# Kernel optimization log

Hardware: AMD Instinct MI355X
Metric: run time of the kernel (lower is better)

Reference implementation:

```python
import jax, jax.numpy as jnp
import numpy as np

B, C, S, H, W = 1, 256, 64, 32, 128
BLOCKS, HEADS, DH = 2, 8, 32
SCALE = DH ** (-0.5)


def layer_norm(x, w, b, eps=1e-5):
    mu = jnp.mean(x, axis=-1, keepdims=True)
    var = jnp.var(x, axis=-1, keepdims=True)
    return (x - mu) * jax.lax.rsqrt(var + eps) * w + b


def generate_y_for_attn(y, u):
    # y: (B,C,H,W), u: (B,S,S) float -> (B, S^2, 2H, C)
    Bv, Cv, Hv, Wv = y.shape
    Sv = u.shape[1]
    uf = jnp.floor(u).reshape(Bv, Sv * Sv)
    u_left = jnp.clip(uf, 0, Wv - 1).astype(jnp.int32)
    u_right = jnp.clip(uf + 1, 0, Wv - 1).astype(jnp.int32)
    yf = y.reshape(Bv, Cv * Hv, Wv)

    def gather_w(idx):
        idxb = jnp.broadcast_to(idx[:, None, :], (Bv, Cv * Hv, Sv * Sv))
        return jnp.take_along_axis(yf, idxb, axis=2).reshape(Bv, Cv, Hv, Sv * Sv)

    ys = jnp.concatenate([gather_w(u_left), gather_w(u_right)], axis=2)  # (B,C,2H,S2)
    return ys.transpose(0, 3, 2, 1)  # (B, S2, 2H, C)


def cross_attention(x, y, p, i):
    # x: (B,M,C), y: (B,M,N,C)
    q = layer_norm(x, p['ln_q_w'][i], p['ln_q_b'][i]) @ p['Wq'][i]        # (B,M,HD)
    k = layer_norm(y, p['ln_k_w'][i], p['ln_k_b'][i]) @ p['Wk'][i]        # (B,M,N,HD)
    v = layer_norm(y, p['ln_v_w'][i], p['ln_v_b'][i]) @ p['Wv'][i]        # (B,M,N,HD)
    Bv, M, _ = q.shape
    N = k.shape[2]
    q = q.reshape(Bv, M, HEADS, DH)
    k = k.reshape(Bv, M, N, HEADS, DH)
    v = v.reshape(Bv, M, N, HEADS, DH)
    dot = SCALE * jnp.einsum('bmhd,bmnhd->bhmn', q, k)                    # (B,H,M,N)
    attn = jax.nn.softmax(dot, axis=-1)
    a = jnp.einsum('bhmn,bmnhd->bmhd', attn, v).reshape(Bv, M, HEADS * DH)
    z = a @ p['Wproj'][i] + p['bproj'][i]
    z = layer_norm(z, p['ln_pre_w'][i], p['ln_pre_b'][i])
    h = jax.nn.gelu(z @ p['Wm1'][i] + p['bm1'][i], approximate=False)
    z = z + (h @ p['Wm2'][i] + p['bm2'][i])
    return layer_norm(z, p['ln_post_w'][i], p['ln_post_b'][i])


def setup_inputs() -> dict:
    key = jax.random.key(0)
    ks = jax.random.split(key, 16)
    std = 0.02
    inp = {
        'grd2sat': jax.random.normal(ks[0], (B, C, S, S), jnp.float32),
        'grd_x': jax.random.normal(ks[1], (B, C, H, W), jnp.float32),
        'u': jax.random.uniform(ks[2], (B, S, S), jnp.float32) * (W - 1),
        'ln_q_w': jnp.ones((BLOCKS, C)), 'ln_q_b': jnp.zeros((BLOCKS, C)),
        'ln_k_w': jnp.ones((BLOCKS, C)), 'ln_k_b': jnp.zeros((BLOCKS, C)),
        'ln_v_w': jnp.ones((BLOCKS, C)), 'ln_v_b': jnp.zeros((BLOCKS, C)),
        'Wq': std * jax.random.normal(ks[3], (BLOCKS, C, HEADS * DH)),
        'Wk': std * jax.random.normal(ks[4], (BLOCKS, C, HEADS * DH)),
        'Wv': std * jax.random.normal(ks[5], (BLOCKS, C, HEADS * DH)),
        'Wproj': std * jax.random.normal(ks[6], (BLOCKS, HEADS * DH, C)),
        'bproj': jnp.zeros((BLOCKS, C)),
        'ln_pre_w': jnp.ones((BLOCKS, C)), 'ln_pre_b': jnp.zeros((BLOCKS, C)),
        'Wm1': std * jax.random.normal(ks[7], (BLOCKS, C, 2 * C)),
        'bm1': jnp.zeros((BLOCKS, 2 * C)),
        'Wm2': std * jax.random.normal(ks[8], (BLOCKS, 2 * C, C)),
        'bm2': jnp.zeros((BLOCKS, C)),
        'ln_post_w': jnp.ones((BLOCKS, C)), 'ln_post_b': jnp.zeros((BLOCKS, C)),
    }
    return inp


def reference(grd2sat, grd_x, u, ln_q_w, ln_q_b, ln_k_w, ln_k_b, ln_v_w, ln_v_b,
              Wq, Wk, Wv, Wproj, bproj, ln_pre_w, ln_pre_b, Wm1, bm1, Wm2, bm2,
              ln_post_w, ln_post_b):
    p = dict(ln_q_w=ln_q_w, ln_q_b=ln_q_b, ln_k_w=ln_k_w, ln_k_b=ln_k_b,
             ln_v_w=ln_v_w, ln_v_b=ln_v_b, Wq=Wq, Wk=Wk, Wv=Wv, Wproj=Wproj,
             bproj=bproj, ln_pre_w=ln_pre_w, ln_pre_b=ln_pre_b, Wm1=Wm1, bm1=bm1,
             Wm2=Wm2, bm2=bm2, ln_post_w=ln_post_w, ln_post_b=ln_post_b)
    y_attn = generate_y_for_attn(grd_x, u)               # (B, S^2, 2H, C)
    x = grd2sat.reshape(B, C, S * S).transpose(0, 2, 1)  # (B, M, C)
    for i in range(BLOCKS):
        # (Swin self-attention layer omitted; cross-attention stack only.)
        x = cross_attention(x, y_attn, p, i)
    out = x.transpose(0, 2, 1).reshape(B, C, S, S)
    # L2 normalize over channel dim
    norm = jnp.sqrt(jnp.sum(out * out, axis=1, keepdims=True))
    return out / jnp.maximum(norm, 1e-12)
```

## Files before the change

### kernel.cpp

```cpp
#include <hip/hip_runtime.h>
#include <math.h>


#define C_DIM 256
#define M_DIM 4096
#define W_DIM 128
#define H_DIM 32
#define ATT_SCALE 0.17677669529663687f

typedef __attribute__((ext_vector_type(8))) short short8;
typedef __attribute__((ext_vector_type(4))) short short4v;
typedef __attribute__((ext_vector_type(4))) float floatx4;

__device__ __forceinline__ unsigned short f2bf(float f) {
    unsigned u = __float_as_uint(f);
    unsigned r = (u + 0x7fffu + ((u >> 16) & 1u)) >> 16;
    return (unsigned short)r;
}
__device__ __forceinline__ float gelu_exact(float x) {
    return 0.5f * x * (1.0f + erff(x * 0.70710678118654752f));
}

struct PrepArgs {
    const float* grd2sat; float* xcur;
    const float* grd_x;   float* yhat;
    const float* u; int* perm; int4* chunks; int* nchunks;
    const float* win[12]; unsigned short* wout[12]; const float* wlnw[12];
    int wR[12], wC[12], wbase[13];
    const float* fW[10]; const float* flnb[10]; const float* fbase[10];
    float* fout[10];
    int fN[10], fwcol[10], focol[10];
};

__global__ __launch_bounds__(256) void prep_kernel(PrepArgs a) {
    __shared__ float smemf[9024];
    int b = blockIdx.x, t = threadIdx.x;
    if (b < 256) {
        float (*tile)[65] = (float(*)[65])smemf;
        int m0 = (b & 63) << 6, c0 = (b >> 6) << 6;
        for (int it = 0; it < 16; ++it) {
            int idx = it * 256 + t;
            int co = idx >> 6, mo = idx & 63;
            tile[co][mo] = a.grd2sat[(size_t)(c0 + co) * M_DIM + m0 + mo];
        }
        __syncthreads();
        for (int it = 0; it < 16; ++it) {
            int idx = it * 256 + t;
            int mo = idx >> 6, co = idx & 63;
            a.xcur[(size_t)(m0 + mo) * C_DIM + c0 + co] = tile[co][mo];
        }
    } else if (b < 384) {
        int idx = b - 256;
        int h = idx & 31, w0 = (idx >> 5) << 5;
        float (*tile)[33] = (float(*)[33])smemf;
        float (*ps)[32] = (float(*)[32])(smemf + 8448);
        float (*pss)[32] = (float(*)[32])(smemf + 8704);
        float* mu_s = smemf + 8960;
        float* rs_s = smemf + 8992;
        int wo = t & 31, cb = t >> 5;
        for (int it = 0; it < 32; ++it) {
            int c = it * 8 + cb;
            tile[c][wo] = a.grd_x[(size_t)c * (H_DIM * W_DIM) + h * W_DIM + w0 + wo];
        }
        __syncthreads();
        {
            int w = t & 31, part = t >> 5;
            float s = 0.f, ss = 0.f;
            for (int c = part * 32; c < part * 32 + 32; ++c) {
                float x = tile[c][w];
                s += x; ss += x * x;
            }
            ps[part][w] = s; pss[part][w] = ss;
        }
        __syncthreads();
        if (t < 32) {
            float s = 0.f, ss = 0.f;
            for (int p = 0; p < 8; ++p) { s += ps[p][t]; ss += pss[p][t]; }
            float mu = s * (1.f / 256.f);
            float var = ss * (1.f / 256.f) - mu * mu;
            mu_s[t] = mu;
            rs_s[t] = rsqrtf(var + 1e-5f);
        }
        __syncthreads();
        for (int jj = 0; jj < 32; ++jj) {
            float mu = mu_s[jj], rs = rs_s[jj];
            a.yhat[((size_t)(w0 + jj) * H_DIM + h) * C_DIM + t] =
                (tile[t][jj] - mu) * rs;
        }
    } else if (b < 1408) {
        int wI = b - 384;
        int e = 0;
        while (wI >= a.wbase[e + 1]) ++e;
        int tl = wI - a.wbase[e];
        int tilesC = a.wC[e] >> 5;
        int tr = tl / tilesC, tc = tl - tr * tilesC;
        int r0 = tr << 5, c0 = tc << 5;
        const float* in = a.win[e];
        unsigned short* out = a.wout[e];
        const float* lnw = a.wlnw[e];
        int R = a.wR[e], Cc = a.wC[e];
        float (*tile)[33] = (float(*)[33])smemf;
        int rl = t >> 3, cq = (t & 7) << 2;
        float4 v = *(const float4*)&in[(size_t)(r0 + rl) * Cc + c0 + cq];
        if (lnw) {
            float s = lnw[r0 + rl];
            v.x *= s; v.y *= s; v.z *= s; v.w *= s;
        }
        tile[rl][cq + 0] = v.x;
        tile[rl][cq + 1] = v.y;
        tile[rl][cq + 2] = v.z;
        tile[rl][cq + 3] = v.w;
        __syncthreads();
        int cl = t >> 3, rq = (t & 7) << 2;
        ushort4 o;
        o.x = f2bf(tile[rq + 0][cl]);
        o.y = f2bf(tile[rq + 1][cl]);
        o.z = f2bf(tile[rq + 2][cl]);
        o.w = f2bf(tile[rq + 3][cl]);
        *(ushort4*)&out[(size_t)(c0 + cl) * R + r0 + rq] = o;
    } else if (b < 1448) {
        int idx = b - 1408;
        int jj = idx >> 2, part = idx & 3;
        int N = a.fN[jj];
        int c = t & 63, kp = t >> 6;
        int wcol = a.fwcol[jj] + (part << 6) + c;
        const float* W = a.fW[jj];
        const float* lb = a.flnb[jj];
        float s = 0.f;
        for (int k = kp * 64; k < kp * 64 + 64; ++k)
            s += lb[k] * W[(size_t)k * N + wcol];
        smemf[(kp << 6) + c] = s;
        __syncthreads();
        if (t < 64) {
            float tot = smemf[t] + smemf[64 + t] + smemf[128 + t] + smemf[192 + t];
            int ocol = a.focol[jj] + (part << 6) + t;
            if (a.fbase[jj]) tot += a.fbase[jj][a.fwcol[jj] + (part << 6) + t];
            a.fout[jj][ocol] = tot;
        }
    } else {
        int* hist = (int*)smemf;
        int* cur = (int*)smemf + 128;
        unsigned short* wlb = (unsigned short*)((int*)smemf + 256);
        if (t < 128) hist[t] = 0;
        __syncthreads();
        for (int it = 0; it < 16; ++it) {
            int m = it * 256 + t;
            int wl = (int)floorf(a.u[m]);
            wl = max(0, min(wl, 126));
            wlb[m] = (unsigned short)wl;
            atomicAdd(&hist[wl], 1);
        }
        __syncthreads();
        if (t == 0) {
            int run = 0, nc = 0;
            for (int bkt = 0; bkt < 127; ++bkt) {
                int c = hist[bkt];
                cur[bkt] = run;
                int q0 = run;
                while (c > 0) {
                    int take = min(c, 32);
                    a.chunks[nc] = make_int4(bkt, q0, take, 0);
                    ++nc; q0 += take; c -= take;
                }
                run += hist[bkt];
            }
            *a.nchunks = nc;
        }
        __syncthreads();
        for (int it = 0; it < 16; ++it) {
            int m = it * 256 + t;
            int wl = wlb[m];
            int pos = atomicAdd(&cur[wl], 1);
            a.perm[pos] = m;
        }
    }
}

struct GJ {
    const void* A; const unsigned short* Bt;
    const float* bias;
    void* out; unsigned short* out2;
    int K, N;
};

__device__ __forceinline__ void gemm_core_kv(const GJ& j, short (*As)[264],
                                             short (*Bs)[264], int bm, int by) {
    int t = threadIdx.x;
    int bn = by << 6;
    int wv = t >> 6, lane = t & 63;
    int mt = wv & 1, nt0 = (wv >> 1) << 1;
    int quad = lane >> 4, l16 = lane & 15;
    floatx4 acc0 = {0.f, 0.f, 0.f, 0.f};
    floatx4 acc1 = {0.f, 0.f, 0.f, 0.f};
    {
        int ar = t >> 3, cq = (t & 7) << 2;
        const float* ap = (const float*)j.A + (size_t)(bm + ar) * 256 + cq;
        float4 v[8];
#pragma unroll
        for (int g = 0; g < 8; ++g) v[g] = *(const float4*)(ap + g * 32);
#pragma unroll
        for (int g = 0; g < 8; ++g) {
            short4v o;
            o[0] = (short)f2bf(v[g].x);
            o[1] = (short)f2bf(v[g].y);
            o[2] = (short)f2bf(v[g].z);
            o[3] = (short)f2bf(v[g].w);
            *(short4v*)&As[ar][cq + g * 32] = o;
        }
    }
    {
        int br = t >> 2, cq2 = (t & 3) << 3;
        const unsigned short* bp = j.Bt + (size_t)(bn + br) * 256 + cq2;
#pragma unroll
        for (int g = 0; g < 8; ++g)
            *(short8*)&Bs[br][cq2 + g * 32] = *(const short8*)(bp + g * 32);
    }
    __syncthreads();
#pragma unroll
    for (int k0 = 0; k0 < 8; ++k0) {
        short8 aa = *(const short8*)&As[(mt << 4) + l16][(k0 << 5) + (quad << 3)];
        short8 b0 = *(const short8*)&Bs[(nt0 << 4) + l16][(k0 << 5) + (quad << 3)];
        short8 b1 =
            *(const short8*)&Bs[((nt0 + 1) << 4) + l16][(k0 << 5) + (quad << 3)];
        acc0 = __builtin_amdgcn_mfma_f32_16x16x32_bf16(aa, b0, acc0, 0, 0, 0);
        acc1 = __builtin_amdgcn_mfma_f32_16x16x32_bf16(aa, b1, acc1, 0, 0, 0);
    }
#pragma unroll
    for (int jj = 0; jj < 2; ++jj) {
        const floatx4 accv = jj ? acc1 : acc0;
        int col = bn + ((nt0 + jj) << 4) + l16;
        float bv = j.bias[col];
#pragma unroll
        for (int r = 0; r < 4; ++r) {
            int row = bm + (mt << 4) + (quad << 2) + r;
            float v = accv[r] + bv;
            if (col < 256)
                ((unsigned short*)j.out)[(size_t)row * 256 + col] = f2bf(v);
            else
                j.out2[(size_t)(col - 256) * M_DIM + row] = f2bf(v);
        }
    }
}

__global__ __launch_bounds__(256) void kv_kernel(GJ j0, GJ j1) {
    __shared__ short As[32][264];
    __shared__ short Bs[64][264];
    int bm = blockIdx.x << 5;
    if ((int)blockIdx.y < 8)
        gemm_core_kv(j0, As, Bs, bm, blockIdx.y);
    else
        gemm_core_kv(j1, As, Bs, bm, blockIdx.y - 8);
}

struct MegaArgs {
    const float* xcur;
    const int* perm; const int4* chunks; const int* nchunks;
    float* xfinal;
    const unsigned short* Wq[2]; const unsigned short* Wp[2];
    const unsigned short* Wm1[2]; const unsigned short* Wm2[2];
    const unsigned short* Ktb[2]; const unsigned short* Vtb[2];
    const float* qb[2]; const float* m1b[2];
    const float* bpj[2]; const float* bm2v[2];
    const float* pw[2]; const float* pb[2];
    const float* aw; const float* ab;
};

struct BPre { short8 b[8][2]; };

__device__ __forceinline__ void preloadB(const unsigned short* Bt, int Kstride,
                                         int koff, int colw, int l16, int quad,
                                         BPre& P) {
    const unsigned short* bp =
        Bt + (size_t)(colw + l16) * Kstride + koff + (quad << 3);
#pragma unroll
    for (int k0 = 0; k0 < 8; ++k0)
#pragma unroll
        for (int ni = 0; ni < 2; ++ni)
            P.b[k0][ni] =
                *(const short8*)(bp + (size_t)(ni << 4) * Kstride + (k0 << 5));
}

__device__ __forceinline__ void mfma32t(const short* As, int lda, const BPre& P,
                                        int l16, int quad, floatx4 acc[2][2]) {
    const short* ap = As + (size_t)l16 * lda + (quad << 3);
#pragma unroll
    for (int k0 = 0; k0 < 8; ++k0) {
        short8 a0 = *(const short8*)(ap + (k0 << 5));
        short8 a1 = *(const short8*)(ap + (size_t)16 * lda + (k0 << 5));
        acc[0][0] = __builtin_amdgcn_mfma_f32_16x16x32_bf16(a0, P.b[k0][0], acc[0][0], 0, 0, 0);
        acc[0][1] = __builtin_amdgcn_mfma_f32_16x16x32_bf16(a0, P.b[k0][1], acc[0][1], 0, 0, 0);
        acc[1][0] = __builtin_amdgcn_mfma_f32_16x16x32_bf16(a1, P.b[k0][0], acc[1][0], 0, 0, 0);
        acc[1][1] = __builtin_amdgcn_mfma_f32_16x16x32_bf16(a1, P.b[k0][1], acc[1][1], 0, 0, 0);
    }
}

#define ZACC(A) \
    { A[0][0] = (floatx4){0.f,0.f,0.f,0.f}; A[0][1] = (floatx4){0.f,0.f,0.f,0.f}; \
      A[1][0] = (floatx4){0.f,0.f,0.f,0.f}; A[1][1] = (floatx4){0.f,0.f,0.f,0.f}; }

__global__ __launch_bounds__(512) void mega_kernel(MegaArgs a) {
    __shared__ __align__(16) char smem[137856];
    short (*XH)[264] = (short(*)[264])(smem);
    short (*QR)[264] = (short(*)[264])(smem + 16896);
    short (*ZH)[264] = (short(*)[264])(smem + 33792);
    short (*AR)[264] = (short(*)[264])(smem + 50688);
    float (*Zf)[260] = (float(*)[260])(smem + 67584);
    short (*PB)[32][72] = (short(*)[32][72])(smem + 100864);
    int* gp = (int*)(smem + 137728);

    if ((int)blockIdx.x >= *a.nchunks) return;
    int4 cd = a.chunks[blockIdx.x];
    int wl = cd.x, qstart = cd.y, qcnt = cd.z;
    int t = threadIdx.x;
    if (t < 32) gp[t] = (t < qcnt) ? a.perm[qstart + t] : a.perm[qstart];
    __syncthreads();

    int wv = t >> 6, lane = t & 63, quad = lane >> 4, l16 = lane & 15;
    int colw = wv << 5;
    int r16 = t >> 4, c0 = (t & 15) << 4;

#pragma unroll 1
    for (int l = 0; l < 2; ++l) {
        BPre Pq;
        preloadB(a.Wq[l], 256, 0, colw, l16, quad, Pq);
        {
            float4 v[4];
            if (l == 0) {
                const float* xp = a.xcur + (size_t)gp[r16] * 256 + c0;
#pragma unroll
                for (int g4 = 0; g4 < 4; ++g4)
                    v[g4] = *(const float4*)(xp + (g4 << 2));
            } else {
#pragma unroll
                for (int g4 = 0; g4 < 4; ++g4)
                    v[g4] = *(const float4*)&Zf[r16][c0 + (g4 << 2)];
            }
            float s = 0.f, ss = 0.f;
#pragma unroll
            for (int g4 = 0; g4 < 4; ++g4) {
                s += v[g4].x + v[g4].y + v[g4].z + v[g4].w;
                ss += v[g4].x * v[g4].x + v[g4].y * v[g4].y + v[g4].z * v[g4].z +
                      v[g4].w * v[g4].w;
            }
#pragma unroll
            for (int o = 1; o < 16; o <<= 1) {
                s += __shfl_xor(s, o, 64);
                ss += __shfl_xor(ss, o, 64);
            }
            float mu = s * (1.f / 256.f);
            float rs = rsqrtf(ss * (1.f / 256.f) - mu * mu + 1e-5f);
#pragma unroll
            for (int g4 = 0; g4 < 4; ++g4) {
                v[g4].x = (v[g4].x - mu) * rs;
                v[g4].y = (v[g4].y - mu) * rs;
                v[g4].z = (v[g4].z - mu) * rs;
                v[g4].w = (v[g4].w - mu) * rs;
            }
            if (l == 1) {
                float s2 = 0.f, ss2 = 0.f;
#pragma unroll
                for (int g4 = 0; g4 < 4; ++g4) {
                    float4 w4 = *(const float4*)&a.aw[c0 + (g4 << 2)];
                    float4 b4 = *(const float4*)&a.ab[c0 + (g4 << 2)];
                    v[g4].x = v[g4].x * w4.x + b4.x;
                    v[g4].y = v[g4].y * w4.y + b4.y;
                    v[g4].z = v[g4].z * w4.z + b4.z;
                    v[g4].w = v[g4].w * w4.w + b4.w;
                    s2 += v[g4].x + v[g4].y + v[g4].z + v[g4].w;
                    ss2 += v[g4].x * v[g4].x + v[g4].y * v[g4].y +
                           v[g4].z * v[g4].z + v[g4].w * v[g4].w;
                }
#pragma unroll
                for (int o = 1; o < 16; o <<= 1) {
                    s2 += __shfl_xor(s2, o, 64);
                    ss2 += __shfl_xor(ss2, o, 64);
                }
                float mu2 = s2 * (1.f / 256.f);
                float rs2 = rsqrtf(ss2 * (1.f / 256.f) - mu2 * mu2 + 1e-5f);
#pragma unroll
                for (int g4 = 0; g4 < 4; ++g4) {
                    v[g4].x = (v[g4].x - mu2) * rs2;
                    v[g4].y = (v[g4].y - mu2) * rs2;
                    v[g4].z = (v[g4].z - mu2) * rs2;
                    v[g4].w = (v[g4].w - mu2) * rs2;
                }
            }
#pragma unroll
            for (int g4 = 0; g4 < 4; ++g4) {
                short4v o;
                o[0] = (short)f2bf(v[g4].x);
                o[1] = (short)f2bf(v[g4].y);
                o[2] = (short)f2bf(v[g4].z);
                o[3] = (short)f2bf(v[g4].w);
                *(short4v*)&XH[r16][c0 + (g4 << 2)] = o;
            }
        }
        __syncthreads();

        short8 kb[4], vfrag[2][2];
        {
            const unsigned short* Kt = a.Ktb[l];
            const unsigned short* Vt = a.Vtb[l];
            int h = wv;
#pragma unroll
            for (int nt = 0; nt < 4; ++nt)
                kb[nt] = *(const short8*)(
                    Kt + (size_t)((wl << 5) + (nt << 4) + l16) * 256 +
                    (h << 5) + (quad << 3));
#pragma unroll
            for (int ks = 0; ks < 2; ++ks)
#pragma unroll
                for (int dt = 0; dt < 2; ++dt)
                    vfrag[ks][dt] = *(const short8*)(
                        Vt + (size_t)((h << 5) + (dt << 4) + l16) * M_DIM +
                        (wl << 5) + (ks << 5) + (quad << 3));
        }
        {
            floatx4 acc[2][2];
            ZACC(acc);
            mfma32t((const short*)XH, 264, Pq, l16, quad, acc);
            const float* qb = a.qb[l];
#pragma unroll
            for (int ni = 0; ni < 2; ++ni) {
                int col = colw + (ni << 4) + l16;
                float bv = qb[col];
#pragma unroll
                for (int mi = 0; mi < 2; ++mi)
#pragma unroll
                    for (int r = 0; r < 4; ++r)
                        QR[(mi << 4) + (quad << 2) + r][col] =
                            (short)f2bf(acc[mi][ni][r] + bv);
            }
        }
        __syncthreads();

        BPre Pp;
        {
            int h = wv;
            short8 aq0 = *(const short8*)&QR[l16][(h << 5) + (quad << 3)];
            short8 aq1 = *(const short8*)&QR[16 + l16][(h << 5) + (quad << 3)];
            floatx4 c[2][4];
#pragma unroll
            for (int nt = 0; nt < 4; ++nt) {
                floatx4 z = {0.f, 0.f, 0.f, 0.f};
                c[0][nt] = __builtin_amdgcn_mfma_f32_16x16x32_bf16(aq0, kb[nt], z, 0, 0, 0);
                c[1][nt] = __builtin_amdgcn_mfma_f32_16x16x32_bf16(aq1, kb[nt], z, 0, 0, 0);
            }
            floatx4 ri[2];
#pragma unroll
            for (int m = 0; m < 2; ++m) {
#pragma unroll
                for (int nt = 0; nt < 4; ++nt) {
                    floatx4 e;
#pragma unroll
                    for (int r = 0; r < 4; ++r)
                        e[r] = __expf(c[m][nt][r] * ATT_SCALE);
                    c[m][nt] = e;
                }
                floatx4 s4 = c[m][0] + c[m][1] + c[m][2] + c[m][3];
#pragma unroll
                for (int r = 0; r < 4; ++r) {
                    float s = s4[r];
                    s += __shfl_xor(s, 1, 64);
                    s += __shfl_xor(s, 2, 64);
                    s += __shfl_xor(s, 4, 64);
                    s += __shfl_xor(s, 8, 64);
                    ri[m][r] = 1.f / s;
                }
            }
#pragma unroll
            for (int m = 0; m < 2; ++m)
#pragma unroll
                for (int nt = 0; nt < 4; ++nt)
#pragma unroll
                    for (int r = 0; r < 4; ++r)
                        PB[wv][(m << 4) + (quad << 2) + r][(nt << 4) + l16] =
                            (short)f2bf(c[m][nt][r] * ri[m][r]);
            __threadfence_block();
            preloadB(a.Wp[l], 256, 0, colw, l16, quad, Pp);
            floatx4 o[2][2];
#pragma unroll
            for (int m = 0; m < 2; ++m)
#pragma unroll
                for (int dt = 0; dt < 2; ++dt)
                    o[m][dt] = (floatx4){0.f, 0.f, 0.f, 0.f};
#pragma unroll
            for (int ks = 0; ks < 2; ++ks) {
                short8 pa0 =
                    *(const short8*)&PB[wv][l16][(ks << 5) + (quad << 3)];
                short8 pa1 =
                    *(const short8*)&PB[wv][16 + l16][(ks << 5) + (quad << 3)];
#pragma unroll
                for (int dt = 0; dt < 2; ++dt) {
                    o[0][dt] = __builtin_amdgcn_mfma_f32_16x16x32_bf16(
                        pa0, vfrag[ks][dt], o[0][dt], 0, 0, 0);
                    o[1][dt] = __builtin_amdgcn_mfma_f32_16x16x32_bf16(
                        pa1, vfrag[ks][dt], o[1][dt], 0, 0, 0);
                }
            }
            int h5 = wv << 5;
#pragma unroll
            for (int m = 0; m < 2; ++m)
#pragma unroll
                for (int dt = 0; dt < 2; ++dt)
#pragma unroll
                    for (int r = 0; r < 4; ++r)
                        AR[(m << 4) + (quad << 2) + r]
                          [h5 + (dt << 4) + l16] = (short)f2bf(o[m][dt][r]);
        }
        __syncthreads();

        {
            floatx4 acc[2][2];
            ZACC(acc);
            mfma32t((const short*)AR, 264, Pp, l16, quad, acc);
            const float* bpj = a.bpj[l];
#pragma unroll
            for (int ni = 0; ni < 2; ++ni) {
                int col = colw + (ni << 4) + l16;
                float bv = bpj[col];
#pragma unroll
                for (int mi = 0; mi < 2; ++mi)
#pragma unroll
                    for (int r = 0; r < 4; ++r)
                        Zf[(mi << 4) + (quad << 2) + r][col] = acc[mi][ni][r] + bv;
            }
        }
        __syncthreads();

        BPre Pm1a;
        preloadB(a.Wm1[l], 256, 0, colw, l16, quad, Pm1a);
        {
            const float* pw = a.pw[l];
            const float* pb = a.pb[l];
            float4 v[4];
#pragma unroll
            for (int g4 = 0; g4 < 4; ++g4)
                v[g4] = *(const float4*)&Zf[r16][c0 + (g4 << 2)];
            float s = 0.f, ss = 0.f;
#pragma unroll
            for (int g4 = 0; g4 < 4; ++g4) {
                s += v[g4].x + v[g4].y + v[g4].z + v[g4].w;
                ss += v[g4].x * v[g4].x + v[g4].y * v[g4].y + v[g4].z * v[g4].z +
                      v[g4].w * v[g4].w;
            }
#pragma unroll
            for (int o = 1; o < 16; o <<= 1) {
                s += __shfl_xor(s, o, 64);
                ss += __shfl_xor(ss, o, 64);
            }
            float mu = s * (1.f / 256.f);
            float rs = rsqrtf(ss * (1.f / 256.f) - mu * mu + 1e-5f);
#pragma unroll
            for (int g4 = 0; g4 < 4; ++g4) {
                float4 z;
                z.x = (v[g4].x - mu) * rs;
                z.y = (v[g4].y - mu) * rs;
                z.z = (v[g4].z - mu) * rs;
                z.w = (v[g4].w - mu) * rs;
                short4v o;
                o[0] = (short)f2bf(z.x);
                o[1] = (short)f2bf(z.y);
                o[2] = (short)f2bf(z.z);
                o[3] = (short)f2bf(z.w);
                *(short4v*)&ZH[r16][c0 + (g4 << 2)] = o;
                float4 w4 = *(const float4*)&pw[c0 + (g4 << 2)];
                float4 b4 = *(const float4*)&pb[c0 + (g4 << 2)];
                float4 za;
                za.x = z.x * w4.x + b4.x;
                za.y = z.y * w4.y + b4.y;
                za.z = z.z * w4.z + b4.z;
                za.w = z.w * w4.w + b4.w;
                *(float4*)&Zf[r16][c0 + (g4 << 2)] = za;
            }
        }
        __syncthreads();

        const float* m1b = a.m1b[l];
        BPre Pm2a;
        {
            floatx4 acc[2][2];
            ZACC(acc);
            mfma32t((const short*)ZH, 264, Pm1a, l16, quad, acc);
            BPre Pm1b;
            preloadB(a.Wm1[l] + (size_t)256 * 256, 256, 0, colw, l16, quad, Pm1b);
#pragma unroll
            for (int ni = 0; ni < 2; ++ni) {
                int col = colw + (ni << 4) + l16;
                float bv = m1b[col];
#pragma unroll
                for (int mi = 0; mi < 2; ++mi)
#pragma unroll
                    for (int r = 0; r < 4; ++r)
                        XH[(mi << 4) + (quad << 2) + r][col] =
                            (short)f2bf(gelu_exact(acc[mi][ni][r] + bv));
            }
            floatx4 acc2[2][2];
            ZACC(acc2);
            mfma32t((const short*)ZH, 264, Pm1b, l16, quad, acc2);
            preloadB(a.Wm2[l], 512, 0, colw, l16, quad, Pm2a);
#pragma unroll
            for (int ni = 0; ni < 2; ++ni) {
                int col = colw + (ni << 4) + l16;
                float bv = m1b[256 + col];
#pragma unroll
                for (int mi = 0; mi < 2; ++mi)
#pragma unroll
                    for (int r = 0; r < 4; ++r)
                        QR[(mi << 4) + (quad << 2) + r][col] =
                            (short)f2bf(gelu_exact(acc2[mi][ni][r] + bv));
            }
        }
        __syncthreads();

        {
            floatx4 macc[2][2];
            ZACC(macc);
            mfma32t((const short*)XH, 264, Pm2a, l16, quad, macc);
            BPre Pm2b;
            preloadB(a.Wm2[l], 512, 256, colw, l16, quad, Pm2b);
            mfma32t((const short*)QR, 264, Pm2b, l16, quad, macc);
            const float* b2 = a.bm2v[l];
#pragma unroll
            for (int ni = 0; ni < 2; ++ni) {
                int col = colw + (ni << 4) + l16;
                float bv = b2[col];
#pragma unroll
                for (int mi = 0; mi < 2; ++mi)
#pragma unroll
                    for (int r = 0; r < 4; ++r) {
                        int row = (mi << 4) + (quad << 2) + r;
                        float v = macc[mi][ni][r] + bv + Zf[row][col];
                        if (l == 0) {
                            Zf[row][col] = v;
                        } else if (row < qcnt) {
                            a.xfinal[(size_t)gp[row] * 256 + col] = v;
                        }
                    }
            }
        }
        __syncthreads();
    }
}

__global__ __launch_bounds__(256) void out_kernel(const float* __restrict__ X,
                                                  const float* __restrict__ w,
                                                  const float* __restrict__ b,
                                                  float* __restrict__ out) {
    __shared__ float tile[64][65];
    int t = threadIdx.x;
    int mo = t >> 2, q = t & 3;
    int m0 = blockIdx.x << 6;
    const float* p = X + (size_t)(m0 + mo) * C_DIM + (q << 6);
    float4 v[16];
    float s = 0.f, ss = 0.f;
#pragma unroll
    for (int c = 0; c < 16; ++c) {
        v[c] = *(const float4*)(p + c * 4);
        s += v[c].x + v[c].y + v[c].z + v[c].w;
        ss += v[c].x * v[c].x + v[c].y * v[c].y + v[c].z * v[c].z + v[c].w * v[c].w;
    }
    s += __shfl_xor(s, 1, 64); s += __shfl_xor(s, 2, 64);
    ss += __shfl_xor(ss, 1, 64); ss += __shfl_xor(ss, 2, 64);
    float mu = s * (1.f / 256.f);
    float rs = rsqrtf(ss * (1.f / 256.f) - mu * mu + 1e-5f);
    float ss2 = 0.f;
#pragma unroll
    for (int c = 0; c < 16; ++c) {
        float4 w4 = *(const float4*)&w[(q << 6) + c * 4];
        float4 b4 = *(const float4*)&b[(q << 6) + c * 4];
        v[c].x = (v[c].x - mu) * rs * w4.x + b4.x;
        v[c].y = (v[c].y - mu) * rs * w4.y + b4.y;
        v[c].z = (v[c].z - mu) * rs * w4.z + b4.z;
        v[c].w = (v[c].w - mu) * rs * w4.w + b4.w;
        ss2 += v[c].x * v[c].x + v[c].y * v[c].y + v[c].z * v[c].z + v[c].w * v[c].w;
    }
    ss2 += __shfl_xor(ss2, 1, 64); ss2 += __shfl_xor(ss2, 2, 64);
    float sc = 1.f / fmaxf(sqrtf(ss2), 1e-12f);
    for (int cc = 0; cc < 4; ++cc) {
        if (q == cc) {
#pragma unroll
            for (int c = 0; c < 16; ++c) {
                tile[mo][c * 4 + 0] = v[c].x * sc;
                tile[mo][c * 4 + 1] = v[c].y * sc;
                tile[mo][c * 4 + 2] = v[c].z * sc;
                tile[mo][c * 4 + 3] = v[c].w * sc;
            }
        }
        __syncthreads();
        for (int it = 0; it < 16; ++it) {
            int idx = it * 256 + t;
            int co = idx >> 6, mr = idx & 63;
            out[(size_t)((cc << 6) + co) * M_DIM + m0 + mr] = tile[mr][co];
        }
        __syncthreads();
    }
}

extern "C" void kernel_launch(void* const* d_in, const int* in_sizes, int n_in,
                              void* d_out, int out_size, void* d_ws, size_t ws_size,
                              hipStream_t stream) {
    const float* grd2sat = (const float*)d_in[0];
    const float* grd_x   = (const float*)d_in[1];
    const float* u       = (const float*)d_in[2];
    const float* ln_q_w  = (const float*)d_in[3];
    const float* ln_q_b  = (const float*)d_in[4];
    const float* ln_k_w  = (const float*)d_in[5];
    const float* ln_k_b  = (const float*)d_in[6];
    const float* ln_v_w  = (const float*)d_in[7];
    const float* ln_v_b  = (const float*)d_in[8];
    const float* Wq      = (const float*)d_in[9];
    const float* Wk      = (const float*)d_in[10];
    const float* Wv      = (const float*)d_in[11];
    const float* Wproj   = (const float*)d_in[12];
    const float* bproj   = (const float*)d_in[13];
    const float* ln_pre_w = (const float*)d_in[14];
    const float* ln_pre_b = (const float*)d_in[15];
    const float* Wm1     = (const float*)d_in[16];
    const float* bm1     = (const float*)d_in[17];
    const float* Wm2     = (const float*)d_in[18];
    const float* bm2     = (const float*)d_in[19];
    const float* ln_post_w = (const float*)d_in[20];
    const float* ln_post_b = (const float*)d_in[21];

    float* ws   = (float*)d_ws;
    float* yhat = ws;
    float* xcur = ws + 1048576;
    float* zq   = ws + 2097152;
    unsigned short* Ktab0 = (unsigned short*)(ws + 6291456);
    unsigned short* Vt0   = (unsigned short*)(ws + 6815744);
    unsigned short* Ktab1 = (unsigned short*)(ws + 7340032);
    unsigned short* Vt1   = (unsigned short*)(ws + 7864320);
    unsigned short* Bt    = (unsigned short*)(ws + 8388608);
    float* biasbuf = ws + 8912896;
    int*  perm    = (int*)(ws + 8915456);
    int4* chunks  = (int4*)(ws + 8919552);
    int*  nchunks = (int*)(ws + 8921600);
    const size_t BS = 524288;
    const size_t OQ = 0, OKV = 65536, OP = 196608, OM1 = 262144, OM2 = 393216;

    dim3 b256(256);

    PrepArgs pa;
    pa.grd2sat = grd2sat; pa.xcur = xcur;
    pa.grd_x = grd_x;     pa.yhat = yhat;
    pa.u = u; pa.perm = perm; pa.chunks = chunks; pa.nchunks = nchunks;
    {
        int base = 0;
        for (int i = 0; i < 2; ++i) {
            int e = 6 * i;
            unsigned short* bt = Bt + i * BS;
            pa.win[e+0] = Wq + i * 65536;    pa.wout[e+0] = bt + OQ;
            pa.wlnw[e+0] = ln_q_w + i * 256; pa.wR[e+0] = 256; pa.wC[e+0] = 256;
            pa.win[e+1] = Wk + i * 65536;    pa.wout[e+1] = bt + OKV;
            pa.wlnw[e+1] = ln_k_w + i * 256; pa.wR[e+1] = 256; pa.wC[e+1] = 256;
            pa.win[e+2] = Wv + i * 65536;    pa.wout[e+2] = bt + OKV + 65536;
            pa.wlnw[e+2] = ln_v_w + i * 256; pa.wR[e+2] = 256; pa.wC[e+2] = 256;
            pa.win[e+3] = Wproj + i * 65536; pa.wout[e+3] = bt + OP;
            pa.wlnw[e+3] = nullptr;          pa.wR[e+3] = 256; pa.wC[e+3] = 256;
            pa.win[e+4] = Wm1 + i * 131072;  pa.wout[e+4] = bt + OM1;
            pa.wlnw[e+4] = ln_pre_w + i * 256; pa.wR[e+4] = 256; pa.wC[e+4] = 512;
            pa.win[e+5] = Wm2 + i * 131072;  pa.wout[e+5] = bt + OM2;
            pa.wlnw[e+5] = nullptr;          pa.wR[e+5] = 512; pa.wC[e+5] = 256;
        }
        for (int e = 0; e < 12; ++e) {
            pa.wbase[e] = base;
            base += (pa.wR[e] >> 5) * (pa.wC[e] >> 5);
        }
        pa.wbase[12] = base;
        for (int i = 0; i < 2; ++i) {
            int jb = 5 * i;
            float* bb = biasbuf + i * 1280;
            pa.fW[jb+0] = Wq + i * 65536; pa.flnb[jb+0] = ln_q_b + i * 256;
            pa.fbase[jb+0] = nullptr; pa.fout[jb+0] = bb;
            pa.fN[jb+0] = 256; pa.fwcol[jb+0] = 0; pa.focol[jb+0] = 0;
            pa.fW[jb+1] = Wk + i * 65536; pa.flnb[jb+1] = ln_k_b + i * 256;
            pa.fbase[jb+1] = nullptr; pa.fout[jb+1] = bb + 256;
            pa.fN[jb+1] = 256; pa.fwcol[jb+1] = 0; pa.focol[jb+1] = 0;
            pa.fW[jb+2] = Wv + i * 65536; pa.flnb[jb+2] = ln_v_b + i * 256;
            pa.fbase[jb+2] = nullptr; pa.fout[jb+2] = bb + 256;
            pa.fN[jb+2] = 256; pa.fwcol[jb+2] = 0; pa.focol[jb+2] = 256;
            pa.fW[jb+3] = Wm1 + i * 131072; pa.flnb[jb+3] = ln_pre_b + i * 256;
            pa.fbase[jb+3] = bm1 + i * 512; pa.fout[jb+3] = bb + 768;
            pa.fN[jb+3] = 512; pa.fwcol[jb+3] = 0; pa.focol[jb+3] = 0;
            pa.fW[jb+4] = Wm1 + i * 131072; pa.flnb[jb+4] = ln_pre_b + i * 256;
            pa.fbase[jb+4] = bm1 + i * 512; pa.fout[jb+4] = bb + 768;
            pa.fN[jb+4] = 512; pa.fwcol[jb+4] = 256; pa.focol[jb+4] = 256;
        }
    }
    prep_kernel<<<1449, b256, 0, stream>>>(pa);

    GJ jkv0 = {};
    jkv0.A = yhat; jkv0.Bt = Bt + OKV; jkv0.bias = biasbuf + 256;
    jkv0.out = Ktab0; jkv0.out2 = Vt0; jkv0.K = 256; jkv0.N = 512;
    GJ jkv1 = {};
    jkv1.A = yhat; jkv1.Bt = Bt + BS + OKV; jkv1.bias = biasbuf + 1280 + 256;
    jkv1.out = Ktab1; jkv1.out2 = Vt1; jkv1.K = 256; jkv1.N = 512;
    kv_kernel<<<dim3(128, 16), b256, 0, stream>>>(jkv0, jkv1);

    MegaArgs ma;
    ma.xcur = xcur; ma.perm = perm; ma.chunks = chunks; ma.nchunks = nchunks;
    ma.xfinal = zq;
    for (int i = 0; i < 2; ++i) {
        const unsigned short* bt = Bt + i * BS;
        ma.Wq[i] = bt + OQ; ma.Wp[i] = bt + OP;
        ma.Wm1[i] = bt + OM1; ma.Wm2[i] = bt + OM2;
        ma.Ktb[i] = i ? Ktab1 : Ktab0; ma.Vtb[i] = i ? Vt1 : Vt0;
        ma.qb[i] = biasbuf + i * 1280;
        ma.m1b[i] = biasbuf + i * 1280 + 768;
        ma.bpj[i] = bproj + i * 256;
        ma.bm2v[i] = bm2 + i * 256;
        ma.pw[i] = ln_pre_w + i * 256;
        ma.pb[i] = ln_pre_b + i * 256;
    }
    ma.aw = ln_post_w; ma.ab = ln_post_b;
    mega_kernel<<<288, dim3(512), 0, stream>>>(ma);

    out_kernel<<<64, b256, 0, stream>>>(zq, ln_post_w + 256, ln_post_b + 256,
                                        (float*)d_out);
}
```

Before: 207.1 us.

## Merge four kernels into one cooperative persistent kernel with grid syncs

Replaces the prep, KV-projection, mega and output kernels with a single cooperative kernel of 240 blocks of 512 threads. Each stage loops over its work units and stages are separated by grid-wide barriers, which removes the separate kernel launches. yhat is also stored as bf16 instead of fp32, halving its memory traffic. The cost is fewer resident blocks for the heavy attention and MLP stage (240 instead of up to 288 chunks), grid-barrier overhead, and stage code re-tiled for 512 threads.

Result: slower. 504.7 us (+143.7%).

```diff
diff --git a/kernel.cpp b/kernel.cpp
--- a/kernel.cpp
+++ b/kernel.cpp
@@ -1,12 +1,14 @@
 #include <hip/hip_runtime.h>
+#include <hip/hip_cooperative_groups.h>
 #include <math.h>
+
+namespace cg = cooperative_groups;
 
 
 #define C_DIM 256
 #define M_DIM 4096
-#define W_DIM 128
-#define H_DIM 32
 #define ATT_SCALE 0.17677669529663687f
+#define NBLK 240
 
 typedef __attribute__((ext_vector_type(8))) short short8;
 typedef __attribute__((ext_vector_type(4))) short short4v;
@@ -23,7 +25,7 @@
 
 struct PrepArgs {
     const float* grd2sat; float* xcur;
-    const float* grd_x;   float* yhat;
+    const float* grd_x;   unsigned short* yhat;
     const float* u; int* perm; int4* chunks; int* nchunks;
     const float* win[12]; unsigned short* wout[12]; const float* wlnw[12];
     int wR[12], wC[12], wbase[13];
@@ -31,226 +33,6 @@
     float* fout[10];
     int fN[10], fwcol[10], focol[10];
 };
-
-__global__ __launch_bounds__(256) void prep_kernel(PrepArgs a) {
-    __shared__ float smemf[9024];
-    int b = blockIdx.x, t = threadIdx.x;
-    if (b < 256) {
-        float (*tile)[65] = (float(*)[65])smemf;
-        int m0 = (b & 63) << 6, c0 = (b >> 6) << 6;
-        for (int it = 0; it < 16; ++it) {
-            int idx = it * 256 + t;
-            int co = idx >> 6, mo = idx & 63;
-            tile[co][mo] = a.grd2sat[(size_t)(c0 + co) * M_DIM + m0 + mo];
-        }
-        __syncthreads();
-        for (int it = 0; it < 16; ++it) {
-            int idx = it * 256 + t;
-            int mo = idx >> 6, co = idx & 63;
-            a.xcur[(size_t)(m0 + mo) * C_DIM + c0 + co] = tile[co][mo];
-        }
-    } else if (b < 384) {
-        int idx = b - 256;
-        int h = idx & 31, w0 = (idx >> 5) << 5;
-        float (*tile)[33] = (float(*)[33])smemf;
-        float (*ps)[32] = (float(*)[32])(smemf + 8448);
-        float (*pss)[32] = (float(*)[32])(smemf + 8704);
-        float* mu_s = smemf + 8960;
-        float* rs_s = smemf + 8992;
-        int wo = t & 31, cb = t >> 5;
-        for (int it = 0; it < 32; ++it) {
-            int c = it * 8 + cb;
-            tile[c][wo] = a.grd_x[(size_t)c * (H_DIM * W_DIM) + h * W_DIM + w0 + wo];
-        }
-        __syncthreads();
-        {
-            int w = t & 31, part = t >> 5;
-            float s = 0.f, ss = 0.f;
-            for (int c = part * 32; c < part * 32 + 32; ++c) {
-                float x = tile[c][w];
-                s += x; ss += x * x;
-            }
-            ps[part][w] = s; pss[part][w] = ss;
-        }
-        __syncthreads();
-        if (t < 32) {
-            float s = 0.f, ss = 0.f;
-            for (int p = 0; p < 8; ++p) { s += ps[p][t]; ss += pss[p][t]; }
-            float mu = s * (1.f / 256.f);
-            float var = ss * (1.f / 256.f) - mu * mu;
-            mu_s[t] = mu;
-            rs_s[t] = rsqrtf(var + 1e-5f);
-        }
-        __syncthreads();
-        for (int jj = 0; jj < 32; ++jj) {
-            float mu = mu_s[jj], rs = rs_s[jj];
-            a.yhat[((size_t)(w0 + jj) * H_DIM + h) * C_DIM + t] =
-                (tile[t][jj] - mu) * rs;
-        }
-    } else if (b < 1408) {
-        int wI = b - 384;
-        int e = 0;
-        while (wI >= a.wbase[e + 1]) ++e;
-        int tl = wI - a.wbase[e];
-        int tilesC = a.wC[e] >> 5;
-        int tr = tl / tilesC, tc = tl - tr * tilesC;
-        int r0 = tr << 5, c0 = tc << 5;
-        const float* in = a.win[e];
-        unsigned short* out = a.wout[e];
-        const float* lnw = a.wlnw[e];
-        int R = a.wR[e], Cc = a.wC[e];
-        float (*tile)[33] = (float(*)[33])smemf;
-        int rl = t >> 3, cq = (t & 7) << 2;
-        float4 v = *(const float4*)&in[(size_t)(r0 + rl) * Cc + c0 + cq];
-        if (lnw) {
-            float s = lnw[r0 + rl];
-            v.x *= s; v.y *= s; v.z *= s; v.w *= s;
-        }
-        tile[rl][cq + 0] = v.x;
-        tile[rl][cq + 1] = v.y;
-        tile[rl][cq + 2] = v.z;
-        tile[rl][cq + 3] = v.w;
-        __syncthreads();
-        int cl = t >> 3, rq = (t & 7) << 2;
-        ushort4 o;
-        o.x = f2bf(tile[rq + 0][cl]);
-        o.y = f2bf(tile[rq + 1][cl]);
-        o.z = f2bf(tile[rq + 2][cl]);
-        o.w = f2bf(tile[rq + 3][cl]);
-        *(ushort4*)&out[(size_t)(c0 + cl) * R + r0 + rq] = o;
-    } else if (b < 1448) {
-        int idx = b - 1408;
-        int jj = idx >> 2, part = idx & 3;
-        int N = a.fN[jj];
-        int c = t & 63, kp = t >> 6;
-        int wcol = a.fwcol[jj] + (part << 6) + c;
-        const float* W = a.fW[jj];
-        const float* lb = a.flnb[jj];
-        float s = 0.f;
-        for (int k = kp * 64; k < kp * 64 + 64; ++k)
-            s += lb[k] * W[(size_t)k * N + wcol];
-        smemf[(kp << 6) + c] = s;
-        __syncthreads();
-        if (t < 64) {
-            float tot = smemf[t] + smemf[64 + t] + smemf[128 + t] + smemf[192 + t];
-            int ocol = a.focol[jj] + (part << 6) + t;
-            if (a.fbase[jj]) tot += a.fbase[jj][a.fwcol[jj] + (part << 6) + t];
-            a.fout[jj][ocol] = tot;
-        }
-    } else {
-        int* hist = (int*)smemf;
-        int* cur = (int*)smemf + 128;
-        unsigned short* wlb = (unsigned short*)((int*)smemf + 256);
-        if (t < 128) hist[t] = 0;
-        __syncthreads();
-        for (int it = 0; it < 16; ++it) {
-            int m = it * 256 + t;
-            int wl = (int)floorf(a.u[m]);
-            wl = max(0, min(wl, 126));
-            wlb[m] = (unsigned short)wl;
-            atomicAdd(&hist[wl], 1);
-        }
-        __syncthreads();
-        if (t == 0) {
-            int run = 0, nc = 0;
-            for (int bkt = 0; bkt < 127; ++bkt) {
-                int c = hist[bkt];
-                cur[bkt] = run;
-                int q0 = run;
-                while (c > 0) {
-                    int take = min(c, 32);
-                    a.chunks[nc] = make_int4(bkt, q0, take, 0);
-                    ++nc; q0 += take; c -= take;
-                }
-                run += hist[bkt];
-            }
-            *a.nchunks = nc;
-        }
-        __syncthreads();
-        for (int it = 0; it < 16; ++it) {
-            int m = it * 256 + t;
-            int wl = wlb[m];
-            int pos = atomicAdd(&cur[wl], 1);
-            a.perm[pos] = m;
-        }
-    }
-}
-
-struct GJ {
-    const void* A; const unsigned short* Bt;
-    const float* bias;
-    void* out; unsigned short* out2;
-    int K, N;
-};
-
-__device__ __forceinline__ void gemm_core_kv(const GJ& j, short (*As)[264],
-                                             short (*Bs)[264], int bm, int by) {
-    int t = threadIdx.x;
-    int bn = by << 6;
-    int wv = t >> 6, lane = t & 63;
-    int mt = wv & 1, nt0 = (wv >> 1) << 1;
-    int quad = lane >> 4, l16 = lane & 15;
-    floatx4 acc0 = {0.f, 0.f, 0.f, 0.f};
-    floatx4 acc1 = {0.f, 0.f, 0.f, 0.f};
-    {
-        int ar = t >> 3, cq = (t & 7) << 2;
-        const float* ap = (const float*)j.A + (size_t)(bm + ar) * 256 + cq;
-        float4 v[8];
-#pragma unroll
-        for (int g = 0; g < 8; ++g) v[g] = *(const float4*)(ap + g * 32);
-#pragma unroll
-        for (int g = 0; g < 8; ++g) {
-            short4v o;
-            o[0] = (short)f2bf(v[g].x);
-            o[1] = (short)f2bf(v[g].y);
-            o[2] = (short)f2bf(v[g].z);
-            o[3] = (short)f2bf(v[g].w);
-            *(short4v*)&As[ar][cq + g * 32] = o;
-        }
-    }
-    {
-        int br = t >> 2, cq2 = (t & 3) << 3;
-        const unsigned short* bp = j.Bt + (size_t)(bn + br) * 256 + cq2;
-#pragma unroll
-        for (int g = 0; g < 8; ++g)
-            *(short8*)&Bs[br][cq2 + g * 32] = *(const short8*)(bp + g * 32);
-    }
-    __syncthreads();
-#pragma unroll
-    for (int k0 = 0; k0 < 8; ++k0) {
-        short8 aa = *(const short8*)&As[(mt << 4) + l16][(k0 << 5) + (quad << 3)];
-        short8 b0 = *(const short8*)&Bs[(nt0 << 4) + l16][(k0 << 5) + (quad << 3)];
-        short8 b1 =
-            *(const short8*)&Bs[((nt0 + 1) << 4) + l16][(k0 << 5) + (quad << 3)];
-        acc0 = __builtin_amdgcn_mfma_f32_16x16x32_bf16(aa, b0, acc0, 0, 0, 0);
-        acc1 = __builtin_amdgcn_mfma_f32_16x16x32_bf16(aa, b1, acc1, 0, 0, 0);
-    }
-#pragma unroll
-    for (int jj = 0; jj < 2; ++jj) {
-        const floatx4 accv = jj ? acc1 : acc0;
-        int col = bn + ((nt0 + jj) << 4) + l16;
-        float bv = j.bias[col];
-#pragma unroll
-        for (int r = 0; r < 4; ++r) {
-            int row = bm + (mt << 4) + (quad << 2) + r;
-            float v = accv[r] + bv;
-            if (col < 256)
-                ((unsigned short*)j.out)[(size_t)row * 256 + col] = f2bf(v);
-            else
-                j.out2[(size_t)(col - 256) * M_DIM + row] = f2bf(v);
-        }
-    }
-}
-
-__global__ __launch_bounds__(256) void kv_kernel(GJ j0, GJ j1) {
-    __shared__ short As[32][264];
-    __shared__ short Bs[64][264];
-    int bm = blockIdx.x << 5;
-    if ((int)blockIdx.y < 8)
-        gemm_core_kv(j0, As, Bs, bm, blockIdx.y);
-    else
-        gemm_core_kv(j1, As, Bs, bm, blockIdx.y - 8);
-}
 
 struct MegaArgs {
     const float* xcur;
@@ -265,6 +47,18 @@
     const float* aw; const float* ab;
 };
 
+struct UberArgs {
+    PrepArgs p;
+    const unsigned short* kvA;
+    const unsigned short* kvBt[2];
+    const float* kvbias[2];
+    unsigned short* kvK[2];
+    unsigned short* kvV[2];
+    MegaArgs m;
+    const float* ow; const float* ob;
+    const float* oX; float* oOut;
+};
+
 struct BPre { short8 b[8][2]; };
 
 __device__ __forceinline__ void preloadB(const unsigned short* Bt, int Kstride,
@@ -298,402 +92,654 @@
     { A[0][0] = (floatx4){0.f,0.f,0.f,0.f}; A[0][1] = (floatx4){0.f,0.f,0.f,0.f}; \
       A[1][0] = (floatx4){0.f,0.f,0.f,0.f}; A[1][1] = (floatx4){0.f,0.f,0.f,0.f}; }
 
-__global__ __launch_bounds__(512) void mega_kernel(MegaArgs a) {
-    __shared__ __align__(16) char smem[137856];
-    short (*XH)[264] = (short(*)[264])(smem);
-    short (*QR)[264] = (short(*)[264])(smem + 16896);
-    short (*ZH)[264] = (short(*)[264])(smem + 33792);
-    short (*AR)[264] = (short(*)[264])(smem + 50688);
-    float (*Zf)[260] = (float(*)[260])(smem + 67584);
-    short (*PB)[32][72] = (short(*)[32][72])(smem + 100864);
-    int* gp = (int*)(smem + 137728);
-
-    if ((int)blockIdx.x >= *a.nchunks) return;
-    int4 cd = a.chunks[blockIdx.x];
-    int wl = cd.x, qstart = cd.y, qcnt = cd.z;
+__global__ __launch_bounds__(512) void uber_kernel(UberArgs a) {
+    __shared__ __align__(16) char smem[138240];
+    cg::grid_group grid = cg::this_grid();
     int t = threadIdx.x;
-    if (t < 32) gp[t] = (t < qcnt) ? a.perm[qstart + t] : a.perm[qstart];
-    __syncthreads();
-
-    int wv = t >> 6, lane = t & 63, quad = lane >> 4, l16 = lane & 15;
-    int colw = wv << 5;
-    int r16 = t >> 4, c0 = (t & 15) << 4;
-
+    int bid = blockIdx.x;
+
+    {
+        float* smemf = (float*)smem;
+        for (int u = bid; u < 1449; u += NBLK) {
+            if (u < 256) {
+                float (*tile)[65] = (float(*)[65])smemf;
+                int m0 = (u & 63) << 6, c0 = (u >> 6) << 6;
+                for (int it = 0; it < 8; ++it) {
+                    int idx = it * 512 + t;
+                    int co = idx >> 6, mo = idx & 63;
+                    tile[co][mo] =
+                        a.p.grd2sat[(size_t)(c0 + co) * M_DIM + m0 + mo];
+                }
+                __syncthreads();
+                for (int it = 0; it < 8; ++it) {
+                    int idx = it * 512 + t;
+                    int mo = idx >> 6, co = idx & 63;
+                    a.p.xcur[(size_t)(m0 + mo) * C_DIM + c0 + co] = tile[co][mo];
+                }
+            } else if (u < 384) {
+                int idx0 = u - 256;
+                int h = idx0 & 31, w0 = (idx0 >> 5) << 5;
+                float (*tile)[33] = (float(*)[33])smemf;
+                float (*ps)[32] = (float(*)[32])(smemf + 8448);
+                float (*pss)[32] = (float(*)[32])(smemf + 8960);
+                float* mu_s = smemf + 9472;
+                float* rs_s = smemf + 9504;
+                int wo = t & 31, cb = t >> 5;
+                for (int it = 0; it < 16; ++it) {
+                    int c = it * 16 + cb;
+                    tile[c][wo] =
+                        a.p.grd_x[(size_t)c * 4096 + h * 128 + w0 + wo];
+                }
+                __syncthreads();
+                {
+                    int w = t & 31, part = t >> 5;
+                    float s = 0.f, ss = 0.f;
+                    for (int c = part * 16; c < part * 16 + 16; ++c) {
+                        float x = tile[c][w];
+                        s += x; ss += x * x;
+                    }
+                    ps[part][w] = s; pss[part][w] = ss;
+                }
+                __syncthreads();
+                if (t < 32) {
+                    float s = 0.f, ss = 0.f;
+                    for (int p = 0; p < 16; ++p) { s += ps[p][t]; ss += pss[p][t]; }
+                    float mu = s * (1.f / 256.f);
+                    float var = ss * (1.f / 256.f) - mu * mu;
+                    mu_s[t] = mu;
+                    rs_s[t] = rsqrtf(var + 1e-5f);
+                }
+                __syncthreads();
+                {
+                    int ch = t & 255;
+                    for (int it = 0; it < 16; ++it) {
+                        int jj = (it << 1) | (t >> 8);
+                        a.p.yhat[((size_t)(w0 + jj) * 32 + h) * C_DIM + ch] =
+                            f2bf((tile[ch][jj] - mu_s[jj]) * rs_s[jj]);
+                    }
+                }
+            } else if (u < 1408) {
+                int wI = u - 384;
+                int e = 0;
+                while (wI >= a.p.wbase[e + 1]) ++e;
+                int tl = wI - a.p.wbase[e];
+                int tilesC = a.p.wC[e] >> 5;
+                int tr = tl / tilesC, tc = tl - tr * tilesC;
+                int r0 = tr << 5, c0 = tc << 5;
+                const float* in = a.p.win[e];
+                unsigned short* out = a.p.wout[e];
+                const float* lnw = a.p.wlnw[e];
+                int R = a.p.wR[e], Cc = a.p.wC[e];
+                float (*tile)[33] = (float(*)[33])smemf;
+                if (t < 256) {
+                    int rl = t >> 3, cq = (t & 7) << 2;
+                    float4 v = *(const float4*)&in[(size_t)(r0 + rl) * Cc + c0 + cq];
+                    if (lnw) {
+                        float s = lnw[r0 + rl];
+                        v.x *= s; v.y *= s; v.z *= s; v.w *= s;
+                    }
+                    tile[rl][cq + 0] = v.x;
+                    tile[rl][cq + 1] = v.y;
+                    tile[rl][cq + 2] = v.z;
+                    tile[rl][cq + 3] = v.w;
+                }
+                __syncthreads();
+                if (t < 256) {
+                    int cl = t >> 3, rq = (t & 7) << 2;
+                    ushort4 o;
+                    o.x = f2bf(tile[rq + 0][cl]);
+                    o.y = f2bf(tile[rq + 1][cl]);
+                    o.z = f2bf(tile[rq + 2][cl]);
+                    o.w = f2bf(tile[rq + 3][cl]);
+                    *(ushort4*)&out[(size_t)(c0 + cl) * R + r0 + rq] = o;
+                }
+            } else if (u < 1448) {
+                int idx0 = u - 1408;
+                int jj = idx0 >> 2, part = idx0 & 3;
+                int N = a.p.fN[jj];
+                int c = t & 63, kp = t >> 6;
+                int wcol = a.p.fwcol[jj] + (part << 6) + c;
+                const float* W = a.p.fW[jj];
+                const float* lb = a.p.flnb[jj];
+                float s = 0.f;
+#pragma unroll 4
+                for (int k = kp * 32; k < kp * 32 + 32; ++k)
+                    s += lb[k] * W[(size_t)k * N + wcol];
+                smemf[(kp << 6) + c] = s;
+                __syncthreads();
+                if (t < 64) {
+                    float tot = 0.f;
+#pragma unroll
+                    for (int p = 0; p < 8; ++p) tot += smemf[(p << 6) + t];
+                    int ocol = a.p.focol[jj] + (part << 6) + t;
+                    if (a.p.fbase[jj])
+                        tot += a.p.fbase[jj][a.p.fwcol[jj] + (part << 6) + t];
+                    a.p.fout[jj][ocol] = tot;
+                }
+            } else {
+                int* hist = (int*)smemf;
+                int* cur = (int*)smemf + 128;
+                unsigned short* wlb = (unsigned short*)((int*)smemf + 256);
+                if (t < 128) hist[t] = 0;
+                __syncthreads();
+                if (t < 256) {
+                    for (int it = 0; it < 16; ++it) {
+                        int m = it * 256 + t;
+                        int wl = (int)floorf(a.p.u[m]);
+                        wl = max(0, min(wl, 126));
+                        wlb[m] = (unsigned short)wl;
+                        atomicAdd(&hist[wl], 1);
+                    }
+                }
+                __syncthreads();
+                if (t == 0) {
+                    int run = 0, nc = 0;
+                    for (int bkt = 0; bkt < 127; ++bkt) {
+                        int c = hist[bkt];
+                        cur[bkt] = run;
+                        int q0 = run;
+                        while (c > 0) {
+                            int take = min(c, 32);
+                            a.p.chunks[nc] = make_int4(bkt, q0, take, 0);
+                            ++nc; q0 += take; c -= take;
+                        }
+                        run += hist[bkt];
+                    }
+                    *a.p.nchunks = nc;
+                }
+                __syncthreads();
+                if (t < 256) {
+                    for (int it = 0; it < 16; ++it) {
+                        int m = it * 256 + t;
+                        int wl = wlb[m];
+                        int pos = atomicAdd(&cur[wl], 1);
+                        a.p.perm[pos] = m;
+                    }
+                }
+            }
+            __syncthreads();
+        }
+    }
+    __threadfence();
+    grid.sync();
+    __threadfence();
+
+    {
+        short (*As)[264] = (short(*)[264])smem;
+        short (*Bs)[264] = (short(*)[264])(smem + 16896);
+        int wv = t >> 6, lane = t & 63, quad = lane >> 4, l16 = lane & 15;
+        int g2 = wv >> 2, wv4 = wv & 3;
+        int mt = wv4 & 1, nt0 = (wv4 >> 1) << 1;
+        int tl = t & 255;
+        for (int u = bid; u < 256; u += NBLK) {
+            int j = u >> 7, bm = (u & 127) << 5;
+            {
+                int ar = t >> 4, cq = (t & 15) << 4;
+                const unsigned short* ap =
+                    a.kvA + (size_t)(bm + ar) * 256 + cq;
+                *(uint4*)&As[ar][cq] = *(const uint4*)(ap);
+                *(uint4*)&As[ar][cq + 8] = *(const uint4*)(ap + 8);
+            }
+            const unsigned short* Bt = a.kvBt[j];
+            const float* bias = a.kvbias[j];
+            unsigned short* Ko = a.kvK[j];
+            unsigned short* Vo = a.kvV[j];
 #pragma unroll 1
-    for (int l = 0; l < 2; ++l) {
-        BPre Pq;
-        preloadB(a.Wq[l], 256, 0, colw, l16, quad, Pq);
-        {
-            float4 v[4];
-            if (l == 0) {
-                const float* xp = a.xcur + (size_t)gp[r16] * 256 + c0;
-#pragma unroll
-                for (int g4 = 0; g4 < 4; ++g4)
-                    v[g4] = *(const float4*)(xp + (g4 << 2));
-            } else {
-#pragma unroll
-                for (int g4 = 0; g4 < 4; ++g4)
-                    v[g4] = *(const float4*)&Zf[r16][c0 + (g4 << 2)];
+            for (int p = 0; p < 4; ++p) {
+                int bn = (p << 7) + (g2 << 6);
+                {
+                    int br = tl >> 2, cq2 = (tl & 3) << 3;
+                    const unsigned short* bp =
+                        Bt + (size_t)(bn + br) * 256 + cq2;
+                    short (*B)[264] = Bs + (size_t)g2 * 64;
+#pragma unroll
+                    for (int g = 0; g < 8; ++g)
+                        *(short8*)&B[br][cq2 + g * 32] =
+                            *(const short8*)(bp + g * 32);
+                }
+                __syncthreads();
+                floatx4 acc0 = {0.f, 0.f, 0.f, 0.f};
+                floatx4 acc1 = {0.f, 0.f, 0.f, 0.f};
+                short (*B)[264] = Bs + (size_t)g2 * 64;
+#pragma unroll
+                for (int k0 = 0; k0 < 8; ++k0) {
+                    short8 aa = *(const short8*)&As[(mt << 4) + l16]
+                                                  [(k0 << 5) + (quad << 3)];
+                    short8 b0 = *(const short8*)&B[(nt0 << 4) + l16]
+                                                 [(k0 << 5) + (quad << 3)];
+                    short8 b1 = *(const short8*)&B[((nt0 + 1) << 4) + l16]
+                                                 [(k0 << 5) + (quad << 3)];
+                    acc0 = __builtin_amdgcn_mfma_f32_16x16x32_bf16(aa, b0, acc0, 0, 0, 0);
+                    acc1 = __builtin_amdgcn_mfma_f32_16x16x32_bf16(aa, b1, acc1, 0, 0, 0);
+                }
+#pragma unroll
+                for (int jj2 = 0; jj2 < 2; ++jj2) {
+                    const floatx4 accv = jj2 ? acc1 : acc0;
+                    int col = bn + ((nt0 + jj2) << 4) + l16;
+                    float bv = bias[col];
+#pragma unroll
+                    for (int r = 0; r < 4; ++r) {
+                        int row = bm + (mt << 4) + (quad << 2) + r;
+                        float v = accv[r] + bv;
+                        if (col < 256)
+                            Ko[(size_t)row * 256 + col] = f2bf(v);
+                        else
+                            Vo[(size_t)(col - 256) * M_DIM + row] = f2bf(v);
+                    }
+                }
+                __syncthreads();
             }
-            float s = 0.f, ss = 0.f;
-#pragma unroll
-            for (int g4 = 0; g4 < 4; ++g4) {
-                s += v[g4].x + v[g4].y + v[g4].z + v[g4].w;
-                ss += v[g4].x * v[g4].x + v[g4].y * v[g4].y + v[g4].z * v[g4].z +
-                      v[g4].w * v[g4].w;
+            __syncthreads();
+        }
+    }
+    __threadfence();
+    grid.sync();
+    __threadfence();
+
+    {
+        short (*XH)[264] = (short(*)[264])(smem);
+        short (*QR)[264] = (short(*)[264])(smem + 16896);
+        short (*ZH)[264] = (short(*)[264])(smem + 33792);
+        short (*AR)[264] = (short(*)[264])(smem + 50688);
+        float (*Zf)[260] = (float(*)[260])(smem + 67584);
+        short (*PB)[32][72] = (short(*)[32][72])(smem + 100864);
+        int* gp = (int*)(smem + 137728);
+
+        int nch = *a.m.nchunks;
+        int wv = t >> 6, lane = t & 63, quad = lane >> 4, l16 = lane & 15;
+        int colw = wv << 5;
+        int r16 = t >> 4, c0 = (t & 15) << 4;
+
+        for (int ch = bid; ch < nch; ch += NBLK) {
+            int4 cd = a.m.chunks[ch];
+            int wl = cd.x, qstart = cd.y, qcnt = cd.z;
+            if (t < 32) gp[t] = (t < qcnt) ? a.m.perm[qstart + t] : a.m.perm[qstart];
+            __syncthreads();
+
+#pragma unroll 1
+            for (int l = 0; l < 2; ++l) {
+                BPre Pq;
+                preloadB(a.m.Wq[l], 256, 0, colw, l16, quad, Pq);
+                {
+                    float4 v[4];
+                    if (l == 0) {
+                        const float* xp = a.m.xcur + (size_t)gp[r16] * 256 + c0;
+#pragma unroll
+                        for (int g4 = 0; g4 < 4; ++g4)
+                            v[g4] = *(const float4*)(xp + (g4 << 2));
+                    } else {
+#pragma unroll
+                        for (int g4 = 0; g4 < 4; ++g4)
+                            v[g4] = *(const float4*)&Zf[r16][c0 + (g4 << 2)];
+                    }
+                    float s = 0.f, ss = 0.f;
+#pragma unroll
+                    for (int g4 = 0; g4 < 4; ++g4) {
+                        s += v[g4].x + v[g4].y + v[g4].z + v[g4].w;
+                        ss += v[g4].x * v[g4].x + v[g4].y * v[g4].y +
+                              v[g4].z * v[g4].z + v[g4].w * v[g4].w;
+                    }
+#pragma unroll
+                    for (int o = 1; o < 16; o <<= 1) {
+                        s += __shfl_xor(s, o, 64);
+                        ss += __shfl_xor(ss, o, 64);
+                    }
+                    float mu = s * (1.f / 256.f);
+                    float rs = rsqrtf(ss * (1.f / 256.f) - mu * mu + 1e-5f);
+#pragma unroll
+                    for (int g4 = 0; g4 < 4; ++g4) {
+                        v[g4].x = (v[g4].x - mu) * rs;
+                        v[g4].y = (v[g4].y - mu) * rs;
+                        v[g4].z = (v[g4].z - mu) * rs;
+                        v[g4].w = (v[g4].w - mu) * rs;
+                    }
+                    if (l == 1) {
+                        float s2 = 0.f, ss2 = 0.f;
+#pragma unroll
+                        for (int g4 = 0; g4 < 4; ++g4) {
+                            float4 w4 = *(const float4*)&a.m.aw[c0 + (g4 << 2)];
+                            float4 b4 = *(const float4*)&a.m.ab[c0 + (g4 << 2)];
+                            v[g4].x = v[g4].x * w4.x + b4.x;
+                            v[g4].y = v[g4].y * w4.y + b4.y;
+                            v[g4].z = v[g4].z * w4.z + b4.z;
+                            v[g4].w = v[g4].w * w4.w + b4.w;
+                            s2 += v[g4].x + v[g4].y + v[g4].z + v[g4].w;
+                            ss2 += v[g4].x * v[g4].x + v[g4].y * v[g4].y +
+                                   v[g4].z * v[g4].z + v[g4].w * v[g4].w;
+                        }
+#pragma unroll
+                        for (int o = 1; o < 16; o <<= 1) {
+                            s2 += __shfl_xor(s2, o, 64);
+                            ss2 += __shfl_xor(ss2, o, 64);
+                        }
+                        float mu2 = s2 * (1.f / 256.f);
+                        float rs2 = rsqrtf(ss2 * (1.f / 256.f) - mu2 * mu2 + 1e-5f);
+#pragma unroll
+                        for (int g4 = 0; g4 < 4; ++g4) {
+                            v[g4].x = (v[g4].x - mu2) * rs2;
+                            v[g4].y = (v[g4].y - mu2) * rs2;
+                            v[g4].z = (v[g4].z - mu2) * rs2;
+                            v[g4].w = (v[g4].w - mu2) * rs2;
+                        }
+                    }
+#pragma unroll
+                    for (int g4 = 0; g4 < 4; ++g4) {
+                        short4v o;
+                        o[0] = (short)f2bf(v[g4].x);
+                        o[1] = (short)f2bf(v[g4].y);
+                        o[2] = (short)f2bf(v[g4].z);
+                        o[3] = (short)f2bf(v[g4].w);
+                        *(short4v*)&XH[r16][c0 + (g4 << 2)] = o;
+                    }
+                }
+                __syncthreads();
+
+                short8 kb[4], vfrag[2][2];
+                {
+                    const unsigned short* Kt = a.m.Ktb[l];
+                    const unsigned short* Vt = a.m.Vtb[l];
+                    int h = wv;
+#pragma unroll
+                    for (int nt = 0; nt < 4; ++nt)
+                        kb[nt] = *(const short8*)(
+                            Kt + (size_t)((wl << 5) + (nt << 4) + l16) * 256 +
+                            (h << 5) + (quad << 3));
+#pragma unroll
+                    for (int ks = 0; ks < 2; ++ks)
+#pragma unroll
+                        for (int dt = 0; dt < 2; ++dt)
+                            vfrag[ks][dt] = *(const short8*)(
+                                Vt + (size_t)((h << 5) + (dt << 4) + l16) * M_DIM +
+                                (wl << 5) + (ks << 5) + (quad << 3));
+                }
+                {
+                    floatx4 acc[2][2];
+                    ZACC(acc);
+                    mfma32t((const short*)XH, 264, Pq, l16, quad, acc);
+                    const float* qb = a.m.qb[l];
+#pragma unroll
+                    for (int ni = 0; ni < 2; ++ni) {
+                        int col = colw + (ni << 4) + l16;
+                        float bv = qb[col];
+#pragma unroll
+                        for (int mi = 0; mi < 2; ++mi)
+#pragma unroll
+                            for (int r = 0; r < 4; ++r)
+                                QR[(mi << 4) + (quad << 2) + r][col] =
+                                    (short)f2bf(acc[mi][ni][r] + bv);
+                    }
+                }
+                __syncthreads();
+
+                BPre Pp;
+                {
+                    int h = wv;
+                    short8 aq0 = *(const short8*)&QR[l16][(h << 5) + (quad << 3)];
+                    short8 aq1 =
+                        *(const short8*)&QR[16 + l16][(h << 5) + (quad << 3)];
+                    floatx4 c[2][4];
+#pragma unroll
+                    for (int nt = 0; nt < 4; ++nt) {
+                        floatx4 z = {0.f, 0.f, 0.f, 0.f};
+                        c[0][nt] = __builtin_amdgcn_mfma_f32_16x16x32_bf16(aq0, kb[nt], z, 0, 0, 0);
+                        c[1][nt] = __builtin_amdgcn_mfma_f32_16x16x32_bf16(aq1, kb[nt], z, 0, 0, 0);
+                    }
+                    floatx4 ri[2];
+#pragma unroll
+                    for (int m = 0; m < 2; ++m) {
+#pragma unroll
+                        for (int nt = 0; nt < 4; ++nt) {
+                            floatx4 e;
+#pragma unroll
+                            for (int r = 0; r < 4; ++r)
+                                e[r] = __expf(c[m][nt][r] * ATT_SCALE);
+                            c[m][nt] = e;
+                        }
+                        floatx4 s4 = c[m][0] + c[m][1] + c[m][2] + c[m][3];
+#pragma unroll
+                        for (int r = 0; r < 4; ++r) {
+                            float s = s4[r];
+                            s += __shfl_xor(s, 1, 64);
+                            s += __shfl_xor(s, 2, 64);
+                            s += __shfl_xor(s, 4, 64);
+                            s += __shfl_xor(s, 8, 64);
+                            ri[m][r] = 1.f / s;
+                        }
+                    }
+#pragma unroll
+                    for (int m = 0; m < 2; ++m)
+#pragma unroll
+                        for (int nt = 0; nt < 4; ++nt)
+#pragma unroll
+                            for (int r = 0; r < 4; ++r)
+                                PB[wv][(m << 4) + (quad << 2) + r]
+                                  [(nt << 4) + l16] =
+                                    (short)f2bf(c[m][nt][r] * ri[m][r]);
+                    __threadfence_block();
+                    preloadB(a.m.Wp[l], 256, 0, colw, l16, quad, Pp);
+                    floatx4 o[2][2];
+#pragma unroll
+                    for (int m = 0; m < 2; ++m)
+#pragma unroll
+                        for (int dt = 0; dt < 2; ++dt)
+                            o[m][dt] = (floatx4){0.f, 0.f, 0.f, 0.f};
+#pragma unroll
+                    for (int ks = 0; ks < 2; ++ks) {
+                        short8 pa0 =
+                            *(const short8*)&PB[wv][l16][(ks << 5) + (quad << 3)];
+                        short8 pa1 = *(const short8*)&PB[wv][16 + l16]
+                                                       [(ks << 5) + (quad << 3)];
+#pragma unroll
+                        for (int dt = 0; dt < 2; ++dt) {
+                            o[0][dt] = __builtin_amdgcn_mfma_f32_16x16x32_bf16(
+                                pa0, vfrag[ks][dt], o[0][dt], 0, 0, 0);
+                            o[1][dt] = __builtin_amdgcn_mfma_f32_16x16x32_bf16(
+                                pa1, vfrag[ks][dt], o[1][dt], 0, 0, 0);
+                        }
+                    }
+                    int h5 = wv << 5;
+#pragma unroll
+                    for (int m = 0; m < 2; ++m)
+#pragma unroll
+                        for (int dt = 0; dt < 2; ++dt)
+#pragma unroll
+                            for (int r = 0; r < 4; ++r)
+                                AR[(m << 4) + (quad << 2) + r]
+                                  [h5 + (dt << 4) + l16] = (short)f2bf(o[m][dt][r]);
+                }
+                __syncthreads();
+
+                {
+                    floatx4 acc[2][2];
+                    ZACC(acc);
+                    mfma32t((const short*)AR, 264, Pp, l16, quad, acc);
+                    const float* bpj = a.m.bpj[l];
+#pragma unroll
+                    for (int ni = 0; ni < 2; ++ni) {
+                        int col = colw + (ni << 4) + l16;
+                        float bv = bpj[col];
+#pragma unroll
+                        for (int mi = 0; mi < 2; ++mi)
+#pragma unroll
+                            for (int r = 0; r < 4; ++r)
+                                Zf[(mi << 4) + (quad << 2) + r][col] =
+                                    acc[mi][ni][r] + bv;
+                    }
+                }
+                __syncthreads();
+
+                BPre Pm1a;
+                preloadB(a.m.Wm1[l], 256, 0, colw, l16, quad, Pm1a);
+                {
+                    const float* pw = a.m.pw[l];
+                    const float* pb = a.m.pb[l];
+                    float4 v[4];
+#pragma unroll
+                    for (int g4 = 0; g4 < 4; ++g4)
+                        v[g4] = *(const float4*)&Zf[r16][c0 + (g4 << 2)];
+                    float s = 0.f, ss = 0.f;
+#pragma unroll
+                    for (int g4 = 0; g4 < 4; ++g4) {
+                        s += v[g4].x + v[g4].y + v[g4].z + v[g4].w;
+                        ss += v[g4].x * v[g4].x + v[g4].y * v[g4].y +
+                              v[g4].z * v[g4].z + v[g4].w * v[g4].w;
+                    }
+#pragma unroll
+                    for (int o = 1; o < 16; o <<= 1) {
+                        s += __shfl_xor(s, o, 64);
+                        ss += __shfl_xor(ss, o, 64);
+                    }
+                    float mu = s * (1.f / 256.f);
+                    float rs = rsqrtf(ss * (1.f / 256.f) - mu * mu + 1e-5f);
+#pragma unroll
+                    for (int g4 = 0; g4 < 4; ++g4) {
+                        float4 z;
+                        z.x = (v[g4].x - mu) * rs;
+                        z.y = (v[g4].y - mu) * rs;
+                        z.z = (v[g4].z - mu) * rs;
+                        z.w = (v[g4].w - mu) * rs;
+                        short4v o;
+                        o[0] = (short)f2bf(z.x);
+                        o[1] = (short)f2bf(z.y);
+                        o[2] = (short)f2bf(z.z);
+                        o[3] = (short)f2bf(z.w);
+                        *(short4v*)&ZH[r16][c0 + (g4 << 2)] = o;
+                        float4 w4 = *(const float4*)&pw[c0 + (g4 << 2)];
+                        float4 b4 = *(const float4*)&pb[c0 + (g4 << 2)];
+                        float4 za;
+                        za.x = z.x * w4.x + b4.x;
+                        za.y = z.y * w4.y + b4.y;
+                        za.z = z.z * w4.z + b4.z;
+                        za.w = z.w * w4.w + b4.w;
+                        *(float4*)&Zf[r16][c0 + (g4 << 2)] = za;
+                    }
+                }
+                __syncthreads();
+
+                const float* m1b = a.m.m1b[l];
+                BPre Pm2a;
+                {
+                    floatx4 acc[2][2];
+                    ZACC(acc);
+                    mfma32t((const short*)ZH, 264, Pm1a, l16, quad, acc);
+                    BPre Pm1b;
+                    preloadB(a.m.Wm1[l] + (size_t)256 * 256, 256, 0, colw, l16,
+                             quad, Pm1b);
+#pragma unroll
+                    for (int ni = 0; ni < 2; ++ni) {
+                        int col = colw + (ni << 4) + l16;
+                        float bv = m1b[col];
+#pragma unroll
+                        for (int mi = 0; mi < 2; ++mi)
+#pragma unroll
+                            for (int r = 0; r < 4; ++r)
+                                XH[(mi << 4) + (quad << 2) + r][col] =
+                                    (short)f2bf(gelu_exact(acc[mi][ni][r] + bv));
+                    }
+                    floatx4 acc2[2][2];
+                    ZACC(acc2);
+                    mfma32t((const short*)ZH, 264, Pm1b, l16, quad, acc2);
+                    preloadB(a.m.Wm2[l], 512, 0, colw, l16, quad, Pm2a);
+#pragma unroll
+                    for (int ni = 0; ni < 2; ++ni) {
+                        int col = colw + (ni << 4) + l16;
+                        float bv = m1b[256 + col];
+#pragma unroll
+                        for (int mi = 0; mi < 2; ++mi)
+#pragma unroll
+                            for (int r = 0; r < 4; ++r)
+                                QR[(mi << 4) + (quad << 2) + r][col] =
+                                    (short)f2bf(gelu_exact(acc2[mi][ni][r] + bv));
+                    }
+                }
+                __syncthreads();
+
+                {
+                    floatx4 macc[2][2];
+                    ZACC(macc);
+                    mfma32t((const short*)XH, 264, Pm2a, l16, quad, macc);
+                    BPre Pm2b;
+                    preloadB(a.m.Wm2[l], 512, 256, colw, l16, quad, Pm2b);
+                    mfma32t((const short*)QR, 264, Pm2b, l16, quad, macc);
+                    const float* b2 = a.m.bm2v[l];
+#pragma unroll
+                    for (int ni = 0; ni < 2; ++ni) {
+                        int col = colw + (ni << 4) + l16;
+                        float bv = b2[col];
+#pragma unroll
+                        for (int mi = 0; mi < 2; ++mi)
+#pragma unroll
+                            for (int r = 0; r < 4; ++r) {
+                                int row = (mi << 4) + (quad << 2) + r;
+                                float v = macc[mi][ni][r] + bv + Zf[row][col];
+                                if (l == 0) {
+                                    Zf[row][col] = v;
+                                } else if (row < qcnt) {
+                                    a.m.xfinal[(size_t)gp[row] * 256 + col] = v;
+                                }
+                            }
+                    }
+                }
+                __syncthreads();
             }
-#pragma unroll
-            for (int o = 1; o < 16; o <<= 1) {
+        }
+    }
+    __threadfence();
+    grid.sync();
+    __threadfence();
+
+    {
+        float (*tile)[257] = (float(*)[257])smem;
+        int r = t >> 5, q = t & 31;
+        for (int rg = bid; rg < 256; rg += NBLK) {
+            int m0 = rg << 4;
+            const float* p = a.oX + (size_t)(m0 + r) * C_DIM + (q << 3);
+            float4 v0 = *(const float4*)(p);
+            float4 v1 = *(const float4*)(p + 4);
+            float s = v0.x + v0.y + v0.z + v0.w + v1.x + v1.y + v1.z + v1.w;
+            float ss = v0.x * v0.x + v0.y * v0.y + v0.z * v0.z + v0.w * v0.w +
+                       v1.x * v1.x + v1.y * v1.y + v1.z * v1.z + v1.w * v1.w;
+#pragma unroll
+            for (int o = 1; o < 32; o <<= 1) {
                 s += __shfl_xor(s, o, 64);
                 ss += __shfl_xor(ss, o, 64);
             }
             float mu = s * (1.f / 256.f);
             float rs = rsqrtf(ss * (1.f / 256.f) - mu * mu + 1e-5f);
-#pragma unroll
-            for (int g4 = 0; g4 < 4; ++g4) {
-                v[g4].x = (v[g4].x - mu) * rs;
-                v[g4].y = (v[g4].y - mu) * rs;
-                v[g4].z = (v[g4].z - mu) * rs;
-                v[g4].w = (v[g4].w - mu) * rs;
+            float4 w0 = *(const float4*)&a.ow[(q << 3)];
+            float4 w1 = *(const float4*)&a.ow[(q << 3) + 4];
+            float4 b0 = *(const float4*)&a.ob[(q << 3)];
+            float4 b1 = *(const float4*)&a.ob[(q << 3) + 4];
+            v0.x = (v0.x - mu) * rs * w0.x + b0.x;
+            v0.y = (v0.y - mu) * rs * w0.y + b0.y;
+            v0.z = (v0.z - mu) * rs * w0.z + b0.z;
+            v0.w = (v0.w - mu) * rs * w0.w + b0.w;
+            v1.x = (v1.x - mu) * rs * w1.x + b1.x;
+            v1.y = (v1.y - mu) * rs * w1.y + b1.y;
+            v1.z = (v1.z - mu) * rs * w1.z + b1.z;
+            v1.w = (v1.w - mu) * rs * w1.w + b1.w;
+            float ss2 = v0.x * v0.x + v0.y * v0.y + v0.z * v0.z + v0.w * v0.w +
+                        v1.x * v1.x + v1.y * v1.y + v1.z * v1.z + v1.w * v1.w;
+#pragma unroll
+            for (int o = 1; o < 32; o <<= 1) ss2 += __shfl_xor(ss2, o, 64);
+            float sc = 1.f / fmaxf(sqrtf(ss2), 1e-12f);
+            tile[r][(q << 3) + 0] = v0.x * sc;
+            tile[r][(q << 3) + 1] = v0.y * sc;
+            tile[r][(q << 3) + 2] = v0.z * sc;
+            tile[r][(q << 3) + 3] = v0.w * sc;
+            tile[r][(q << 3) + 4] = v1.x * sc;
+            tile[r][(q << 3) + 5] = v1.y * sc;
+            tile[r][(q << 3) + 6] = v1.z * sc;
+            tile[r][(q << 3) + 7] = v1.w * sc;
+            __syncthreads();
+#pragma unroll
+            for (int it = 0; it < 8; ++it) {
+                int idx = it * 512 + t;
+                int c = idx >> 4, m = idx & 15;
+                a.oOut[(size_t)c * M_DIM + m0 + m] = tile[m][c];
             }
-            if (l == 1) {
-                float s2 = 0.f, ss2 = 0.f;
-#pragma unroll
-                for (int g4 = 0; g4 < 4; ++g4) {
-                    float4 w4 = *(const float4*)&a.aw[c0 + (g4 << 2)];
-                    float4 b4 = *(const float4*)&a.ab[c0 + (g4 << 2)];
-                    v[g4].x = v[g4].x * w4.x + b4.x;
-                    v[g4].y = v[g4].y * w4.y + b4.y;
-                    v[g4].z = v[g4].z * w4.z + b4.z;
-                    v[g4].w = v[g4].w * w4.w + b4.w;
-                    s2 += v[g4].x + v[g4].y + v[g4].z + v[g4].w;
-                    ss2 += v[g4].x * v[g4].x + v[g4].y * v[g4].y +
-                           v[g4].z * v[g4].z + v[g4].w * v[g4].w;
-                }
-#pragma unroll
-                for (int o = 1; o < 16; o <<= 1) {
-                    s2 += __shfl_xor(s2, o, 64);
-                    ss2 += __shfl_xor(ss2, o, 64);
-                }
-                float mu2 = s2 * (1.f / 256.f);
-                float rs2 = rsqrtf(ss2 * (1.f / 256.f) - mu2 * mu2 + 1e-5f);
-#pragma unroll
-                for (int g4 = 0; g4 < 4; ++g4) {
-                    v[g4].x = (v[g4].x - mu2) * rs2;
-                    v[g4].y = (v[g4].y - mu2) * rs2;
-                    v[g4].z = (v[g4].z - mu2) * rs2;
-                    v[g4].w = (v[g4].w - mu2) * rs2;
-                }
-            }
-#pragma unroll
-            for (int g4 = 0; g4 < 4; ++g4) {
-                short4v o;
-                o[0] = (short)f2bf(v[g4].x);
-                o[1] = (short)f2bf(v[g4].y);
-                o[2] = (short)f2bf(v[g4].z);
-                o[3] = (short)f2bf(v[g4].w);
-                *(short4v*)&XH[r16][c0 + (g4 << 2)] = o;
-            }
+            __syncthreads();
         }
-        __syncthreads();
-
-        short8 kb[4], vfrag[2][2];
-        {
-            const unsigned short* Kt = a.Ktb[l];
-            const unsigned short* Vt = a.Vtb[l];
-            int h = wv;
-#pragma unroll
-            for (int nt = 0; nt < 4; ++nt)
-                kb[nt] = *(const short8*)(
-                    Kt + (size_t)((wl << 5) + (nt << 4) + l16) * 256 +
-                    (h << 5) + (quad << 3));
-#pragma unroll
-            for (int ks = 0; ks < 2; ++ks)
-#pragma unroll
-                for (int dt = 0; dt < 2; ++dt)
-                    vfrag[ks][dt] = *(const short8*)(
-                        Vt + (size_t)((h << 5) + (dt << 4) + l16) * M_DIM +
-                        (wl << 5) + (ks << 5) + (quad << 3));
-        }
-        {
-            floatx4 acc[2][2];
-            ZACC(acc);
-            mfma32t((const short*)XH, 264, Pq, l16, quad, acc);
-            const float* qb = a.qb[l];
-#pragma unroll
-            for (int ni = 0; ni < 2; ++ni) {
-                int col = colw + (ni << 4) + l16;
-                float bv = qb[col];
-#pragma unroll
-                for (int mi = 0; mi < 2; ++mi)
-#pragma unroll
-                    for (int r = 0; r < 4; ++r)
-                        QR[(mi << 4) + (quad << 2) + r][col] =
-                            (short)f2bf(acc[mi][ni][r] + bv);
-            }
-        }
-        __syncthreads();
-
-        BPre Pp;
-        {
-            int h = wv;
-            short8 aq0 = *(const short8*)&QR[l16][(h << 5) + (quad << 3)];
-            short8 aq1 = *(const short8*)&QR[16 + l16][(h << 5) + (quad << 3)];
-            floatx4 c[2][4];
-#pragma unroll
-            for (int nt = 0; nt < 4; ++nt) {
-                floatx4 z = {0.f, 0.f, 0.f, 0.f};
-                c[0][nt] = __builtin_amdgcn_mfma_f32_16x16x32_bf16(aq0, kb[nt], z, 0, 0, 0);
-                c[1][nt] = __builtin_amdgcn_mfma_f32_16x16x32_bf16(aq1, kb[nt], z, 0, 0, 0);
-            }
-            floatx4 ri[2];
-#pragma unroll
-            for (int m = 0; m < 2; ++m) {
-#pragma unroll
-                for (int nt = 0; nt < 4; ++nt) {
-                    floatx4 e;
-#pragma unroll
-                    for (int r = 0; r < 4; ++r)
-                        e[r] = __expf(c[m][nt][r] * ATT_SCALE);
-                    c[m][nt] = e;
-                }
-                floatx4 s4 = c[m][0] + c[m][1] + c[m][2] + c[m][3];
-#pragma unroll
-                for (int r = 0; r < 4; ++r) {
-                    float s = s4[r];
-                    s += __shfl_xor(s, 1, 64);
-                    s += __shfl_xor(s, 2, 64);
-                    s += __shfl_xor(s, 4, 64);
-                    s += __shfl_xor(s, 8, 64);
-                    ri[m][r] = 1.f / s;
-                }
-            }
-#pragma unroll
-            for (int m = 0; m < 2; ++m)
-#pragma unroll
-                for (int nt = 0; nt < 4; ++nt)
-#pragma unroll
-                    for (int r = 0; r < 4; ++r)
-                        PB[wv][(m << 4) + (quad << 2) + r][(nt << 4) + l16] =
-                            (short)f2bf(c[m][nt][r] * ri[m][r]);
-            __threadfence_block();
-            preloadB(a.Wp[l], 256, 0, colw, l16, quad, Pp);
-            floatx4 o[2][2];
-#pragma unroll
-            for (int m = 0; m < 2; ++m)
-#pragma unroll
-                for (int dt = 0; dt < 2; ++dt)
-                    o[m][dt] = (floatx4){0.f, 0.f, 0.f, 0.f};
-#pragma unroll
-            for (int ks = 0; ks < 2; ++ks) {
-                short8 pa0 =
-                    *(const short8*)&PB[wv][l16][(ks << 5) + (quad << 3)];
-                short8 pa1 =
-                    *(const short8*)&PB[wv][16 + l16][(ks << 5) + (quad << 3)];
-#pragma unroll
-                for (int dt = 0; dt < 2; ++dt) {
-                    o[0][dt] = __builtin_amdgcn_mfma_f32_16x16x32_bf16(
-                        pa0, vfrag[ks][dt], o[0][dt], 0, 0, 0);
-                    o[1][dt] = __builtin_amdgcn_mfma_f32_16x16x32_bf16(
-                        pa1, vfrag[ks][dt], o[1][dt], 0, 0, 0);
-                }
-            }
-            int h5 = wv << 5;
-#pragma unroll
-            for (int m = 0; m < 2; ++m)
-#pragma unroll
-                for (int dt = 0; dt < 2; ++dt)
-#pragma unroll
-                    for (int r = 0; r < 4; ++r)
-                        AR[(m << 4) + (quad << 2) + r]
-                          [h5 + (dt << 4) + l16] = (short)f2bf(o[m][dt][r]);
-        }
-        __syncthreads();
-
-        {
-            floatx4 acc[2][2];
-            ZACC(acc);
-            mfma32t((const short*)AR, 264, Pp, l16, quad, acc);
-            const float* bpj = a.bpj[l];
-#pragma unroll
-            for (int ni = 0; ni < 2; ++ni) {
-                int col = colw + (ni << 4) + l16;
-                float bv = bpj[col];
-#pragma unroll
-                for (int mi = 0; mi < 2; ++mi)
-#pragma unroll
-                    for (int r = 0; r < 4; ++r)
-                        Zf[(mi << 4) + (quad << 2) + r][col] = acc[mi][ni][r] + bv;
-            }
-        }
-        __syncthreads();
-
-        BPre Pm1a;
-        preloadB(a.Wm1[l], 256, 0, colw, l16, quad, Pm1a);
-        {
-            const float* pw = a.pw[l];
-            const float* pb = a.pb[l];
-            float4 v[4];
-#pragma unroll
-            for (int g4 = 0; g4 < 4; ++g4)
-                v[g4] = *(const float4*)&Zf[r16][c0 + (g4 << 2)];
-            float s = 0.f, ss = 0.f;
-#pragma unroll
-            for (int g4 = 0; g4 < 4; ++g4) {
-                s += v[g4].x + v[g4].y + v[g4].z + v[g4].w;
-                ss += v[g4].x * v[g4].x + v[g4].y * v[g4].y + v[g4].z * v[g4].z +
-                      v[g4].w * v[g4].w;
-            }
-#pragma unroll
-            for (int o = 1; o < 16; o <<= 1) {
-                s += __shfl_xor(s, o, 64);
-                ss += __shfl_xor(ss, o, 64);
-            }
-            float mu = s * (1.f / 256.f);
-            float rs = rsqrtf(ss * (1.f / 256.f) - mu * mu + 1e-5f);
-#pragma unroll
-            for (int g4 = 0; g4 < 4; ++g4) {
-                float4 z;
-                z.x = (v[g4].x - mu) * rs;
-                z.y = (v[g4].y - mu) * rs;
-                z.z = (v[g4].z - mu) * rs;
-                z.w = (v[g4].w - mu) * rs;
-                short4v o;
-                o[0] = (short)f2bf(z.x);
-                o[1] = (short)f2bf(z.y);
-                o[2] = (short)f2bf(z.z);
-                o[3] = (short)f2bf(z.w);
-                *(short4v*)&ZH[r16][c0 + (g4 << 2)] = o;
-                float4 w4 = *(const float4*)&pw[c0 + (g4 << 2)];
-                float4 b4 = *(const float4*)&pb[c0 + (g4 << 2)];
-                float4 za;
-                za.x = z.x * w4.x + b4.x;
-                za.y = z.y * w4.y + b4.y;
-                za.z = z.z * w4.z + b4.z;
-                za.w = z.w * w4.w + b4.w;
-                *(float4*)&Zf[r16][c0 + (g4 << 2)] = za;
-            }
-        }
-        __syncthreads();
-
-        const float* m1b = a.m1b[l];
-        BPre Pm2a;
-        {
-            floatx4 acc[2][2];
-            ZACC(acc);
-            mfma32t((const short*)ZH, 264, Pm1a, l16, quad, acc);
-            BPre Pm1b;
-            preloadB(a.Wm1[l] + (size_t)256 * 256, 256, 0, colw, l16, quad, Pm1b);
-#pragma unroll
-            for (int ni = 0; ni < 2; ++ni) {
-                int col = colw + (ni << 4) + l16;
-                float bv = m1b[col];
-#pragma unroll
-                for (int mi = 0; mi < 2; ++mi)
-#pragma unroll
-                    for (int r = 0; r < 4; ++r)
-                        XH[(mi << 4) + (quad << 2) + r][col] =
-                            (short)f2bf(gelu_exact(acc[mi][ni][r] + bv));
-            }
-            floatx4 acc2[2][2];
-            ZACC(acc2);
-            mfma32t((const short*)ZH, 264, Pm1b, l16, quad, acc2);
-            preloadB(a.Wm2[l], 512, 0, colw, l16, quad, Pm2a);
-#pragma unroll
-            for (int ni = 0; ni < 2; ++ni) {
-                int col = colw + (ni << 4) + l16;
-                float bv = m1b[256 + col];
-#pragma unroll
-                for (int mi = 0; mi < 2; ++mi)
-#pragma unroll
-                    for (int r = 0; r < 4; ++r)
-                        QR[(mi << 4) + (quad << 2) + r][col] =
-                            (short)f2bf(gelu_exact(acc2[mi][ni][r] + bv));
-            }
-        }
-        __syncthreads();
-
-        {
-            floatx4 macc[2][2];
-            ZACC(macc);
-            mfma32t((const short*)XH, 264, Pm2a, l16, quad, macc);
-            BPre Pm2b;
-            preloadB(a.Wm2[l], 512, 256, colw, l16, quad, Pm2b);
-            mfma32t((const short*)QR, 264, Pm2b, l16, quad, macc);
-            const float* b2 = a.bm2v[l];
-#pragma unroll
-            for (int ni = 0; ni < 2; ++ni) {
-                int col = colw + (ni << 4) + l16;
-                float bv = b2[col];
-#pragma unroll
-                for (int mi = 0; mi < 2; ++mi)
-#pragma unroll
-                    for (int r = 0; r < 4; ++r) {
-                        int row = (mi << 4) + (quad << 2) + r;
-                        float v = macc[mi][ni][r] + bv + Zf[row][col];
-                        if (l == 0) {
-                            Zf[row][col] = v;
-                        } else if (row < qcnt) {
-                            a.xfinal[(size_t)gp[row] * 256 + col] = v;
-                        }
-                    }
-            }
-        }
-        __syncthreads();
-    }
-}
-
-__global__ __launch_bounds__(256) void out_kernel(const float* __restrict__ X,
-                                                  const float* __restrict__ w,
-                                                  const float* __restrict__ b,
-                                                  float* __restrict__ out) {
-    __shared__ float tile[64][65];
-    int t = threadIdx.x;
-    int mo = t >> 2, q = t & 3;
-    int m0 = blockIdx.x << 6;
-    const float* p = X + (size_t)(m0 + mo) * C_DIM + (q << 6);
-    float4 v[16];
-    float s = 0.f, ss = 0.f;
-#pragma unroll
-    for (int c = 0; c < 16; ++c) {
-        v[c] = *(const float4*)(p + c * 4);
-        s += v[c].x + v[c].y + v[c].z + v[c].w;
-        ss += v[c].x * v[c].x + v[c].y * v[c].y + v[c].z * v[c].z + v[c].w * v[c].w;
-    }
-    s += __shfl_xor(s, 1, 64); s += __shfl_xor(s, 2, 64);
-    ss += __shfl_xor(ss, 1, 64); ss += __shfl_xor(ss, 2, 64);
-    float mu = s * (1.f / 256.f);
-    float rs = rsqrtf(ss * (1.f / 256.f) - mu * mu + 1e-5f);
-    float ss2 = 0.f;
-#pragma unroll
-    for (int c = 0; c < 16; ++c) {
-        float4 w4 = *(const float4*)&w[(q << 6) + c * 4];
-        float4 b4 = *(const float4*)&b[(q << 6) + c * 4];
-        v[c].x = (v[c].x - mu) * rs * w4.x + b4.x;
-        v[c].y = (v[c].y - mu) * rs * w4.y + b4.y;
-        v[c].z = (v[c].z - mu) * rs * w4.z + b4.z;
-        v[c].w = (v[c].w - mu) * rs * w4.w + b4.w;
-        ss2 += v[c].x * v[c].x + v[c].y * v[c].y + v[c].z * v[c].z + v[c].w * v[c].w;
-    }
-    ss2 += __shfl_xor(ss2, 1, 64); ss2 += __shfl_xor(ss2, 2, 64);
-    float sc = 1.f / fmaxf(sqrtf(ss2), 1e-12f);
-    for (int cc = 0; cc < 4; ++cc) {
-        if (q == cc) {
-#pragma unroll
-            for (int c = 0; c < 16; ++c) {
-                tile[mo][c * 4 + 0] = v[c].x * sc;
-                tile[mo][c * 4 + 1] = v[c].y * sc;
-                tile[mo][c * 4 + 2] = v[c].z * sc;
-                tile[mo][c * 4 + 3] = v[c].w * sc;
-            }
-        }
-        __syncthreads();
-        for (int it = 0; it < 16; ++it) {
-            int idx = it * 256 + t;
-            int co = idx >> 6, mr = idx & 63;
-            out[(size_t)((cc << 6) + co) * M_DIM + m0 + mr] = tile[mr][co];
-        }
-        __syncthreads();
     }
 }
 
@@ -724,7 +770,7 @@
     const float* ln_post_b = (const float*)d_in[21];
 
     float* ws   = (float*)d_ws;
-    float* yhat = ws;
+    unsigned short* yhat = (unsigned short*)ws;
     float* xcur = ws + 1048576;
     float* zq   = ws + 2097152;
     unsigned short* Ktab0 = (unsigned short*)(ws + 6291456);
@@ -739,9 +785,8 @@
     const size_t BS = 524288;
     const size_t OQ = 0, OKV = 65536, OP = 196608, OM1 = 262144, OM2 = 393216;
 
-    dim3 b256(256);
-
-    PrepArgs pa;
+    UberArgs ua;
+    PrepArgs& pa = ua.p;
     pa.grd2sat = grd2sat; pa.xcur = xcur;
     pa.grd_x = grd_x;     pa.yhat = yhat;
     pa.u = u; pa.perm = perm; pa.chunks = chunks; pa.nchunks = nchunks;
@@ -788,17 +833,12 @@
             pa.fN[jb+4] = 512; pa.fwcol[jb+4] = 256; pa.focol[jb+4] = 256;
         }
     }
-    prep_kernel<<<1449, b256, 0, stream>>>(pa);
-
-    GJ jkv0 = {};
-    jkv0.A = yhat; jkv0.Bt = Bt + OKV; jkv0.bias = biasbuf + 256;
-    jkv0.out = Ktab0; jkv0.out2 = Vt0; jkv0.K = 256; jkv0.N = 512;
-    GJ jkv1 = {};
-    jkv1.A = yhat; jkv1.Bt = Bt + BS + OKV; jkv1.bias = biasbuf + 1280 + 256;
-    jkv1.out = Ktab1; jkv1.out2 = Vt1; jkv1.K = 256; jkv1.N = 512;
-    kv_kernel<<<dim3(128, 16), b256, 0, stream>>>(jkv0, jkv1);
-
-    MegaArgs ma;
+    ua.kvA = yhat;
+    ua.kvBt[0] = Bt + OKV;       ua.kvBt[1] = Bt + BS + OKV;
+    ua.kvbias[0] = biasbuf + 256; ua.kvbias[1] = biasbuf + 1280 + 256;
+    ua.kvK[0] = Ktab0; ua.kvK[1] = Ktab1;
+    ua.kvV[0] = Vt0;   ua.kvV[1] = Vt1;
+    MegaArgs& ma = ua.m;
     ma.xcur = xcur; ma.perm = perm; ma.chunks = chunks; ma.nchunks = nchunks;
     ma.xfinal = zq;
     for (int i = 0; i < 2; ++i) {
@@ -814,8 +854,10 @@
         ma.pb[i] = ln_pre_b + i * 256;
     }
     ma.aw = ln_post_w; ma.ab = ln_post_b;
-    mega_kernel<<<288, dim3(512), 0, stream>>>(ma);
-
-    out_kernel<<<64, b256, 0, stream>>>(zq, ln_post_w + 256, ln_post_b + 256,
-                                        (float*)d_out);
+    ua.ow = ln_post_w + 256; ua.ob = ln_post_b + 256;
+    ua.oX = zq; ua.oOut = (float*)d_out;
+
+    void* kargs[] = {(void*)&ua};
+    hipLaunchCooperativeKernel((const void*)uber_kernel, dim3(NBLK), dim3(512),
+                               kargs, 0, stream);
 }
```
